# Kernel tuning notes

Hardware: AMD Instinct MI355X
Metric: run time of the kernel (lower is better)

The kernel has to match this reference:

```python
import jax, jax.numpy as jnp
import numpy as np

N_PATIENT = 50000
N_GENE = 20000
N_EDGE = 640000
P_DIM, G_DIM, H, OUT = 64, 32, 128, 8


def setup_inputs() -> dict:
    key = jax.random.key(0)
    ks = jax.random.split(key, 20)
    s = 0.02
    return {
        "x_patient": jax.random.normal(ks[0], (N_PATIENT, P_DIM), jnp.float32),
        "x_gene": jax.random.normal(ks[1], (N_GENE, G_DIM), jnp.float32),
        "edge_index": jax.random.randint(ks[2], (2, N_EDGE), 0, N_GENE, jnp.int32),
        # patient MLP
        "W_p1": jax.random.normal(ks[3], (P_DIM, H), jnp.float32) * s,
        "b_p1": jnp.zeros((H,), jnp.float32),
        "W_p2": jax.random.normal(ks[4], (H, H), jnp.float32) * s,
        "b_p2": jnp.zeros((H,), jnp.float32),
        # gene MLP
        "W_g1": jax.random.normal(ks[5], (G_DIM, H), jnp.float32) * s,
        "b_g1": jnp.zeros((H,), jnp.float32),
        "W_g2": jax.random.normal(ks[6], (H, H), jnp.float32) * s,
        "b_g2": jnp.zeros((H,), jnp.float32),
        # SAGEConv 1: lin_l acts on aggregated src, lin_r (root) on dst
        "W1_l": jax.random.normal(ks[7], (H, H), jnp.float32) * s,
        "b1_l": jnp.zeros((H,), jnp.float32),
        "W1_r": jax.random.normal(ks[8], (H, H), jnp.float32) * s,
        # SAGEConv 2
        "W2_l": jax.random.normal(ks[9], (H, H), jnp.float32) * s,
        "b2_l": jnp.zeros((H,), jnp.float32),
        "W2_r": jax.random.normal(ks[10], (H, H), jnp.float32) * s,
        # final fc
        "W_fc": jax.random.normal(ks[11], (H, OUT), jnp.float32) * s,
        "b_fc": jnp.zeros((OUT,), jnp.float32),
    }


def reference(x_patient, x_gene, edge_index,
              W_p1, b_p1, W_p2, b_p2,
              W_g1, b_g1, W_g2, b_g2,
              W1_l, b1_l, W1_r,
              W2_l, b2_l, W2_r,
              W_fc, b_fc):
    # node-type MLPs
    p = jax.nn.relu(x_patient @ W_p1 + b_p1) @ W_p2 + b_p2   # [N_P, H]
    g = jax.nn.relu(x_gene @ W_g1 + b_g1) @ W_g2 + b_g2       # [N_G, H]

    src, dst = edge_index[0], edge_index[1]
    # gene_x is unchanged between layers, so the sum-aggregate is identical
    # for both SAGEConv layers: compute the gather + segment-sum once.
    agg = jax.ops.segment_sum(g[src], dst, num_segments=x_patient.shape[0])  # [N_P, H]

    # SAGEConv(aggr='sum'): out = lin_l(agg) + lin_r(x_dst), bias in lin_l
    p = jax.nn.relu(agg @ W1_l + b1_l + p @ W1_r)
    p = jax.nn.relu(agg @ W2_l + b2_l + p @ W2_r)
    return p @ W_fc + b_fc  # [N_P, OUT]
```

## Files before the change

kernel.cpp:

```cpp
#include <hip/hip_runtime.h>

#define NP 50000
#define NG 20000
#define NE 640000
#define PD 64
#define GD 32
#define HD 128
#define OD 8
#define CAP 96
#define FILLB 125
#define EPB 5120
#define GENE_TILES 313
#define ROW0_NOAGG 20096
#define PAT2B 234
#define SAGE64B 314
#define AGGPAD (ROW0_NOAGG - NG)

using f32x4 = __attribute__((ext_vector_type(4))) float;
using s16x8 = __attribute__((ext_vector_type(8))) short;

__device__ __forceinline__ unsigned short f2bf(float f) {
    union { float f; unsigned u; } v; v.f = f;
    const unsigned r = v.u + 0x7FFFu + ((v.u >> 16) & 1u);
    return (unsigned short)(r >> 16);
}
__device__ __forceinline__ float bfpair_lo(unsigned v) {
    union { unsigned u; float f; } x; x.u = v << 16; return x.f;
}
__device__ __forceinline__ float bfpair_hi(unsigned v) {
    union { unsigned u; float f; } x; x.u = v & 0xFFFF0000u; return x.f;
}

#define TOT_SWZ 112640

__global__ __launch_bounds__(256) void swz_kernel(
    const float* __restrict__ Wp1, const float* __restrict__ Wp2,
    const float* __restrict__ W1l, const float* __restrict__ W1r,
    const float* __restrict__ W2l, const float* __restrict__ W2r,
    const float* __restrict__ Wfc,
    const float* __restrict__ Wg1, const float* __restrict__ Wg2,
    unsigned short* __restrict__ wswz, unsigned short* __restrict__ aggb)
{
    const int u = blockIdx.x * 256 + threadIdx.x;
    if (u < TOT_SWZ) {
        const float* src; int K, Nr, doff;
        if      (u <   8192) { src = Wp1; K =  64; Nr = HD; doff = 0; }
        else if (u <  24576) { src = Wp2; K = 128; Nr = HD; doff = 8192; }
        else if (u <  40960) { src = W1l; K = 128; Nr = HD; doff = 24576; }
        else if (u <  57344) { src = W1r; K = 128; Nr = HD; doff = 40960; }
        else if (u <  73728) { src = W2l; K = 128; Nr = HD; doff = 57344; }
        else if (u <  90112) { src = W2r; K = 128; Nr = HD; doff = 73728; }
        else if (u <  92160) { src = Wfc; K = 128; Nr = OD; doff = 90112; }
        else if (u <  96256) { src = Wg1; K =  32; Nr = HD; doff = 92160; }
        else                 { src = Wg2; K = 128; Nr = HD; doff = 96256; }
        const int e  = u - doff;
        const int j  = e & 7;
        const int ln = (e >> 3) & 63;
        const int f  = e >> 9;
        const int KC = K >> 5;
        const int c  = f % KC;
        const int n0 = f / KC;
        const int k  = c * 32 + (ln >> 4) * 8 + j;
        const int n  = n0 * 16 + (ln & 15);
        wswz[u] = f2bf((n < Nr) ? src[k * Nr + n] : 0.f);
    } else {
        aggb[(size_t)NG * HD + (u - TOT_SWZ)] = 0;
    }
}

__global__ __launch_bounds__(256) void genefill_kernel(
    const float* __restrict__ xg,
    const unsigned short* __restrict__ wswz,
    const float* __restrict__ bg1, const float* __restrict__ bg2,
    unsigned short* __restrict__ g,
    const int* __restrict__ ei, unsigned short* __restrict__ hist16)
{
    __shared__ __align__(16) char smem[20480];
    const int tid = threadIdx.x;
    if (blockIdx.x >= GENE_TILES) {
        int* cnt = (int*)smem;
#pragma unroll
        for (int k = 0; k < 5; ++k) {
            const int idx = k * 256 + tid;
            if (idx < NG / 16) ((int4*)cnt)[idx] = (int4){0, 0, 0, 0};
        }
        __syncthreads();
        const int fb = blockIdx.x - GENE_TILES;
        const int base = fb * EPB;
#pragma unroll
        for (int it = 0; it < 5; ++it) {
            const int e0 = base + it * 1024 + tid;
            const int d0 = ei[NE + e0];
            const int d1 = ei[NE + e0 + 256];
            const int d2 = ei[NE + e0 + 512];
            const int d3 = ei[NE + e0 + 768];
            atomicAdd(&cnt[d0 >> 2], 1 << ((d0 & 3) * 8));
            atomicAdd(&cnt[d1 >> 2], 1 << ((d1 & 3) * 8));
            atomicAdd(&cnt[d2 >> 2], 1 << ((d2 & 3) * 8));
            atomicAdd(&cnt[d3 >> 2], 1 << ((d3 & 3) * 8));
        }
        __syncthreads();
        unsigned short* Hb = hist16 + fb * NG;
#pragma unroll
        for (int k = 0; k < 20; ++k) {
            const int idx = k * 256 + tid;
            if (idx < NG / 4) {
                const unsigned w = (unsigned)cnt[idx];
                int2 o;
                o.x = (int)((w & 0xFFu) | ((w & 0xFF00u) << 8));
                o.y = (int)(((w >> 16) & 0xFFu) | (((w >> 24) & 0xFFu) << 16));
                ((int2*)Hb)[idx] = o;
            }
        }
        return;
    }
    const unsigned short* wg1 = wswz + 92160;
    const unsigned short* wg2 = wswz + 96256;

    const int lane = tid & 63;
    const int wid  = tid >> 6;
    const int quad = lane >> 4;
    const int l16  = lane & 15;
    const int row0 = blockIdx.x * 64 + wid * 16;
    const int arow = min(row0 + l16, NG - 1);
    unsigned short* X = (unsigned short*)smem + wid * 16 * 136;
    const f32x4 Z = {0.f, 0.f, 0.f, 0.f};

    s16x8 a;
    {
        const float* xr = xg + (size_t)arow * GD + quad * 8;
        const f32x4 u0 = *(const f32x4*)xr;
        const f32x4 u1 = *(const f32x4*)(xr + 4);
#pragma unroll
        for (int j = 0; j < 4; ++j) {
            a[j]     = (short)f2bf(u0[j]);
            a[4 + j] = (short)f2bf(u1[j]);
        }
    }
    f32x4 C[8];
#pragma unroll
    for (int n = 0; n < 8; ++n) {
        const s16x8 b = *(const s16x8*)&wg1[(n * 64 + lane) * 8];
        C[n] = __builtin_amdgcn_mfma_f32_16x16x32_bf16(a, b, Z, 0, 0, 0);
    }
#pragma unroll
    for (int n = 0; n < 8; ++n) {
        const float bias = bg1[n * 16 + l16];
#pragma unroll
        for (int r = 0; r < 4; ++r)
            X[(quad * 4 + r) * 136 + n * 16 + l16] = f2bf(fmaxf(C[n][r] + bias, 0.f));
    }
    __syncthreads();
    s16x8 pa[4];
#pragma unroll
    for (int c = 0; c < 4; ++c) pa[c] = *(const s16x8*)&X[l16 * 136 + c * 32 + quad * 8];
#pragma unroll
    for (int n = 0; n < 8; ++n) {
        C[n] = Z;
#pragma unroll
        for (int c = 0; c < 4; ++c) {
            const s16x8 b = *(const s16x8*)&wg2[((n * 4 + c) * 64 + lane) * 8];
            C[n] = __builtin_amdgcn_mfma_f32_16x16x32_bf16(pa[c], b, C[n], 0, 0, 0);
        }
    }
#pragma unroll
    for (int n = 0; n < 8; ++n) {
        const float bias = bg2[n * 16 + l16];
#pragma unroll
        for (int r = 0; r < 4; ++r) {
            const int row = row0 + quad * 4 + r;
            if (row < NG) g[(size_t)row * HD + n * 16 + l16] = f2bf(C[n][r] + bias);
        }
    }
}

__global__ __launch_bounds__(256) void scan_kernel(
    unsigned short* __restrict__ hist16, int* __restrict__ cursor)
{
    const int d = blockIdx.x * 256 + threadIdx.x;
    if (d >= NG) return;
    int run = 0;
#pragma unroll 5
    for (int b = 0; b < FILLB; ++b) {
        const int t = hist16[b * NG + d];
        hist16[b * NG + d] = (unsigned short)run;
        run += t;
    }
    cursor[d] = run;
}

__global__ __launch_bounds__(256) void placepat_kernel(
    const int* __restrict__ ei, const unsigned short* __restrict__ hist16,
    unsigned short* __restrict__ pad,
    const float* __restrict__ xp, const unsigned short* __restrict__ wswz,
    const float* __restrict__ bp1, const float* __restrict__ bp2,
    const float* __restrict__ b1l, const float* __restrict__ b2l,
    const float* __restrict__ bfc,
    float* __restrict__ out)
{
    __shared__ __align__(16) char smem[40960];
    const int tid = threadIdx.x;

    if (blockIdx.x < FILLB) {
        int* cnt = (int*)smem;
        const int* Hb = (const int*)(hist16 + blockIdx.x * NG);
#pragma unroll
        for (int k = 0; k < 10; ++k) {
            const int idx = k * 256 + tid;
            if (idx < NG / 8) ((int4*)cnt)[idx] = ((const int4*)Hb)[idx];
        }
        __syncthreads();
        const int base = blockIdx.x * EPB;
#pragma unroll
        for (int it = 0; it < 5; ++it) {
            const int e0 = base + it * 1024 + tid;
            const int s0 = ei[e0];       const int d0 = ei[NE + e0];
            const int s1 = ei[e0 + 256]; const int d1 = ei[NE + e0 + 256];
            const int s2 = ei[e0 + 512]; const int d2 = ei[NE + e0 + 512];
            const int s3 = ei[e0 + 768]; const int d3 = ei[NE + e0 + 768];
            { const int o = atomicAdd(&cnt[d0 >> 1], 1 << ((d0 & 1) * 16));
              const int p = (o >> ((d0 & 1) * 16)) & 0xFFFF;
              if (p < CAP) pad[d0 * CAP + p] = (unsigned short)s0; }
            { const int o = atomicAdd(&cnt[d1 >> 1], 1 << ((d1 & 1) * 16));
              const int p = (o >> ((d1 & 1) * 16)) & 0xFFFF;
              if (p < CAP) pad[d1 * CAP + p] = (unsigned short)s1; }
            { const int o = atomicAdd(&cnt[d2 >> 1], 1 << ((d2 & 1) * 16));
              const int p = (o >> ((d2 & 1) * 16)) & 0xFFFF;
              if (p < CAP) pad[d2 * CAP + p] = (unsigned short)s2; }
            { const int o = atomicAdd(&cnt[d3 >> 1], 1 << ((d3 & 1) * 16));
              const int p = (o >> ((d3 & 1) * 16)) & 0xFFFF;
              if (p < CAP) pad[d3 * CAP + p] = (unsigned short)s3; }
        }
        return;
    }

    const unsigned short* wp1 = wswz + 0;
    const unsigned short* wp2 = wswz + 8192;
    const unsigned short* w1r = wswz + 40960;
    const unsigned short* w2r = wswz + 73728;
    const unsigned short* wfc = wswz + 90112;

    unsigned short* XA = (unsigned short*)smem;
    const int lane = tid & 63;
    const int wid  = tid >> 6;
    const int quad = lane >> 4;
    const int l16  = lane & 15;
    const int brow = ROW0_NOAGG + (blockIdx.x - FILLB) * 128;
    const int nA = wid * 2, nB = wid * 2 + 1;
    const f32x4 Z = {0.f, 0.f, 0.f, 0.f};

#pragma unroll
    for (int s = 0; s < 8; ++s) {
        const int slot = s * 256 + tid;
        const int r  = slot >> 4;
        const int cv = slot & 15;
        const f32x4 u = *(const f32x4*)&xp[(size_t)min(brow + r, NP - 1) * PD + cv * 4];
        unsigned short o[4];
#pragma unroll
        for (int j = 0; j < 4; ++j) o[j] = f2bf(u[j]);
        *(ushort4*)&XA[r * 136 + cv * 4] = *(ushort4*)o;
    }
    __syncthreads();

    f32x4 acc[8][2];

#pragma unroll
    for (int rt = 0; rt < 8; ++rt) { acc[rt][0] = Z; acc[rt][1] = Z; }
#pragma unroll
    for (int c = 0; c < 2; ++c) {
        const s16x8 b0 = *(const s16x8*)&wp1[((nA * 2 + c) * 64 + lane) * 8];
        const s16x8 b1 = *(const s16x8*)&wp1[((nB * 2 + c) * 64 + lane) * 8];
#pragma unroll
        for (int rt = 0; rt < 8; ++rt) {
            const s16x8 a = *(const s16x8*)&XA[(rt * 16 + l16) * 136 + c * 32 + quad * 8];
            acc[rt][0] = __builtin_amdgcn_mfma_f32_16x16x32_bf16(a, b0, acc[rt][0], 0, 0, 0);
            acc[rt][1] = __builtin_amdgcn_mfma_f32_16x16x32_bf16(a, b1, acc[rt][1], 0, 0, 0);
        }
    }
    __syncthreads();
#pragma unroll
    for (int t = 0; t < 2; ++t) {
        const int n = wid * 2 + t;
        const float bias = bp1[n * 16 + l16];
#pragma unroll
        for (int rt = 0; rt < 8; ++rt)
#pragma unroll
            for (int r = 0; r < 4; ++r)
                XA[(rt * 16 + quad * 4 + r) * 136 + n * 16 + l16] =
                    f2bf(fmaxf(acc[rt][t][r] + bias, 0.f));
    }
    __syncthreads();

#pragma unroll
    for (int rt = 0; rt < 8; ++rt) { acc[rt][0] = Z; acc[rt][1] = Z; }
#pragma unroll
    for (int c = 0; c < 4; ++c) {
        const s16x8 b0 = *(const s16x8*)&wp2[((nA * 4 + c) * 64 + lane) * 8];
        const s16x8 b1 = *(const s16x8*)&wp2[((nB * 4 + c) * 64 + lane) * 8];
#pragma unroll
        for (int rt = 0; rt < 8; ++rt) {
            const s16x8 a = *(const s16x8*)&XA[(rt * 16 + l16) * 136 + c * 32 + quad * 8];
            acc[rt][0] = __builtin_amdgcn_mfma_f32_16x16x32_bf16(a, b0, acc[rt][0], 0, 0, 0);
            acc[rt][1] = __builtin_amdgcn_mfma_f32_16x16x32_bf16(a, b1, acc[rt][1], 0, 0, 0);
        }
    }
    __syncthreads();
#pragma unroll
    for (int t = 0; t < 2; ++t) {
        const int n = wid * 2 + t;
        const float bias = bp2[n * 16 + l16];
#pragma unroll
        for (int rt = 0; rt < 8; ++rt)
#pragma unroll
            for (int r = 0; r < 4; ++r)
                XA[(rt * 16 + quad * 4 + r) * 136 + n * 16 + l16] =
                    f2bf(acc[rt][t][r] + bias);
    }
    __syncthreads();

#pragma unroll
    for (int rt = 0; rt < 8; ++rt) { acc[rt][0] = Z; acc[rt][1] = Z; }
#pragma unroll
    for (int c = 0; c < 4; ++c) {
        const s16x8 b0 = *(const s16x8*)&w1r[((nA * 4 + c) * 64 + lane) * 8];
        const s16x8 b1 = *(const s16x8*)&w1r[((nB * 4 + c) * 64 + lane) * 8];
#pragma unroll
        for (int rt = 0; rt < 8; ++rt) {
            const s16x8 a = *(const s16x8*)&XA[(rt * 16 + l16) * 136 + c * 32 + quad * 8];
            acc[rt][0] = __builtin_amdgcn_mfma_f32_16x16x32_bf16(a, b0, acc[rt][0], 0, 0, 0);
            acc[rt][1] = __builtin_amdgcn_mfma_f32_16x16x32_bf16(a, b1, acc[rt][1], 0, 0, 0);
        }
    }
    __syncthreads();
#pragma unroll
    for (int t = 0; t < 2; ++t) {
        const int n = wid * 2 + t;
        const float bias = b1l[n * 16 + l16];
#pragma unroll
        for (int rt = 0; rt < 8; ++rt)
#pragma unroll
            for (int r = 0; r < 4; ++r)
                XA[(rt * 16 + quad * 4 + r) * 136 + n * 16 + l16] =
                    f2bf(fmaxf(acc[rt][t][r] + bias, 0.f));
    }
    __syncthreads();

#pragma unroll
    for (int rt = 0; rt < 8; ++rt) { acc[rt][0] = Z; acc[rt][1] = Z; }
#pragma unroll
    for (int c = 0; c < 4; ++c) {
        const s16x8 b0 = *(const s16x8*)&w2r[((nA * 4 + c) * 64 + lane) * 8];
        const s16x8 b1 = *(const s16x8*)&w2r[((nB * 4 + c) * 64 + lane) * 8];
#pragma unroll
        for (int rt = 0; rt < 8; ++rt) {
            const s16x8 a = *(const s16x8*)&XA[(rt * 16 + l16) * 136 + c * 32 + quad * 8];
            acc[rt][0] = __builtin_amdgcn_mfma_f32_16x16x32_bf16(a, b0, acc[rt][0], 0, 0, 0);
            acc[rt][1] = __builtin_amdgcn_mfma_f32_16x16x32_bf16(a, b1, acc[rt][1], 0, 0, 0);
        }
    }
    __syncthreads();
#pragma unroll
    for (int t = 0; t < 2; ++t) {
        const int n = wid * 2 + t;
        const float bias = b2l[n * 16 + l16];
#pragma unroll
        for (int rt = 0; rt < 8; ++rt)
#pragma unroll
            for (int r = 0; r < 4; ++r)
                XA[(rt * 16 + quad * 4 + r) * 136 + n * 16 + l16] =
                    f2bf(fmaxf(acc[rt][t][r] + bias, 0.f));
    }
    __syncthreads();

    {
        f32x4 co[2] = {Z, Z};
#pragma unroll
        for (int c = 0; c < 4; ++c) {
            const s16x8 b = *(const s16x8*)&wfc[(c * 64 + lane) * 8];
#pragma unroll
            for (int j = 0; j < 2; ++j) {
                const int rt = wid * 2 + j;
                const s16x8 a = *(const s16x8*)&XA[(rt * 16 + l16) * 136 + c * 32 + quad * 8];
                co[j] = __builtin_amdgcn_mfma_f32_16x16x32_bf16(a, b, co[j], 0, 0, 0);
            }
        }
        if (l16 < OD) {
            const float bias = bfc[l16];
#pragma unroll
            for (int j = 0; j < 2; ++j)
#pragma unroll
                for (int r = 0; r < 4; ++r) {
                    const int row = brow + (wid * 2 + j) * 16 + quad * 4 + r;
                    if (row < NP) out[(size_t)row * OD + l16] = co[j][r] + bias;
                }
        }
    }
}

__global__ __launch_bounds__(256) void agg_kernel(
    const int* __restrict__ cursor, const unsigned short* __restrict__ pad,
    const unsigned short* __restrict__ g, unsigned short* __restrict__ aggb)
{
    const int row  = blockIdx.x * 4 + (threadIdx.x >> 6);
    const int lane = threadIdx.x & 63;
    const int grp  = lane >> 4;
    const int sub  = lane & 15;

    float acc[8] = {0.f, 0.f, 0.f, 0.f, 0.f, 0.f, 0.f, 0.f};
    const int cnt = min(cursor[row], CAP);
    const size_t rb = (size_t)row * CAP;
    for (int i = grp * 4; i < cnt; i += 16) {
        const ushort4 q = *(const ushort4*)&pad[rb + i];
        int r0 = q.x, r1 = q.y, r2 = q.z, r3 = q.w;
        const bool v1 = (i + 1) < cnt, v2 = (i + 2) < cnt, v3 = (i + 3) < cnt;
        r1 = v1 ? r1 : r0;  r2 = v2 ? r2 : r0;  r3 = v3 ? r3 : r0;
        const float s1 = v1 ? 1.f : 0.f, s2 = v2 ? 1.f : 0.f, s3 = v3 ? 1.f : 0.f;
        const s16x8 g0 = *(const s16x8*)&g[(size_t)r0 * HD + sub * 8];
        const s16x8 g1 = *(const s16x8*)&g[(size_t)r1 * HD + sub * 8];
        const s16x8 g2 = *(const s16x8*)&g[(size_t)r2 * HD + sub * 8];
        const s16x8 g3 = *(const s16x8*)&g[(size_t)r3 * HD + sub * 8];
        const unsigned* d0 = (const unsigned*)&g0;
        const unsigned* d1 = (const unsigned*)&g1;
        const unsigned* d2 = (const unsigned*)&g2;
        const unsigned* d3 = (const unsigned*)&g3;
#pragma unroll
        for (int k = 0; k < 4; ++k) {
            acc[2 * k]     += bfpair_lo(d0[k]);
            acc[2 * k + 1] += bfpair_hi(d0[k]);
            acc[2 * k]     = fmaf(bfpair_lo(d1[k]), s1, acc[2 * k]);
            acc[2 * k + 1] = fmaf(bfpair_hi(d1[k]), s1, acc[2 * k + 1]);
            acc[2 * k]     = fmaf(bfpair_lo(d2[k]), s2, acc[2 * k]);
            acc[2 * k + 1] = fmaf(bfpair_hi(d2[k]), s2, acc[2 * k + 1]);
            acc[2 * k]     = fmaf(bfpair_lo(d3[k]), s3, acc[2 * k]);
            acc[2 * k + 1] = fmaf(bfpair_hi(d3[k]), s3, acc[2 * k + 1]);
        }
    }
#pragma unroll
    for (int k = 0; k < 8; ++k) {
        acc[k] += __shfl_xor(acc[k], 16);
        acc[k] += __shfl_xor(acc[k], 32);
    }
    if (lane < 16) {
        unsigned o[4];
#pragma unroll
        for (int k = 0; k < 4; ++k)
            o[k] = (unsigned)f2bf(acc[2 * k]) | ((unsigned)f2bf(acc[2 * k + 1]) << 16);
        *(int4*)&aggb[(size_t)row * HD + lane * 8] = *(int4*)o;
    }
}

__global__ __launch_bounds__(256) void sage64_kernel(
    const float* __restrict__ xp, const unsigned short* __restrict__ aggb,
    const unsigned short* __restrict__ wswz,
    const float* __restrict__ bp1, const float* __restrict__ bp2,
    const float* __restrict__ b1l, const float* __restrict__ b2l,
    const float* __restrict__ bfc,
    float* __restrict__ out)
{
    const unsigned short* wp1 = wswz + 0;
    const unsigned short* wp2 = wswz + 8192;
    const unsigned short* w1l = wswz + 24576;
    const unsigned short* w1r = wswz + 40960;
    const unsigned short* w2l = wswz + 57344;
    const unsigned short* w2r = wswz + 73728;
    const unsigned short* wfc = wswz + 90112;

    __shared__ __align__(16) unsigned short XA[64 * 136];

    const int tid  = threadIdx.x;
    const int lane = tid & 63;
    const int wid  = tid >> 6;
    const int quad = lane >> 4;
    const int l16  = lane & 15;
    const int brow = blockIdx.x * 64;
    const int nA = wid * 2, nB = wid * 2 + 1;
    const f32x4 Z = {0.f, 0.f, 0.f, 0.f};

#pragma unroll
    for (int s = 0; s < 4; ++s) {
        const int slot = s * 256 + tid;
        const int r  = slot >> 4;
        const int cv = slot & 15;
        const f32x4 u = *(const f32x4*)&xp[(size_t)(brow + r) * PD + cv * 4];
        unsigned short o[4];
#pragma unroll
        for (int j = 0; j < 4; ++j) o[j] = f2bf(u[j]);
        *(ushort4*)&XA[r * 136 + cv * 4] = *(ushort4*)o;
    }
    __syncthreads();

    f32x4 acc[4][2];

#pragma unroll
    for (int rt = 0; rt < 4; ++rt) { acc[rt][0] = Z; acc[rt][1] = Z; }
#pragma unroll
    for (int c = 0; c < 2; ++c) {
        const s16x8 b0 = *(const s16x8*)&wp1[((nA * 2 + c) * 64 + lane) * 8];
        const s16x8 b1 = *(const s16x8*)&wp1[((nB * 2 + c) * 64 + lane) * 8];
#pragma unroll
        for (int rt = 0; rt < 4; ++rt) {
            const s16x8 a = *(const s16x8*)&XA[(rt * 16 + l16) * 136 + c * 32 + quad * 8];
            acc[rt][0] = __builtin_amdgcn_mfma_f32_16x16x32_bf16(a, b0, acc[rt][0], 0, 0, 0);
            acc[rt][1] = __builtin_amdgcn_mfma_f32_16x16x32_bf16(a, b1, acc[rt][1], 0, 0, 0);
        }
    }
    __syncthreads();
#pragma unroll
    for (int t = 0; t < 2; ++t) {
        const int n = wid * 2 + t;
        const float bias = bp1[n * 16 + l16];
#pragma unroll
        for (int rt = 0; rt < 4; ++rt)
#pragma unroll
            for (int r = 0; r < 4; ++r)
                XA[(rt * 16 + quad * 4 + r) * 136 + n * 16 + l16] =
                    f2bf(fmaxf(acc[rt][t][r] + bias, 0.f));
    }
    __syncthreads();

#pragma unroll
    for (int rt = 0; rt < 4; ++rt) { acc[rt][0] = Z; acc[rt][1] = Z; }
#pragma unroll
    for (int c = 0; c < 4; ++c) {
        const s16x8 b0 = *(const s16x8*)&wp2[((nA * 4 + c) * 64 + lane) * 8];
        const s16x8 b1 = *(const s16x8*)&wp2[((nB * 4 + c) * 64 + lane) * 8];
#pragma unroll
        for (int rt = 0; rt < 4; ++rt) {
            const s16x8 a = *(const s16x8*)&XA[(rt * 16 + l16) * 136 + c * 32 + quad * 8];
            acc[rt][0] = __builtin_amdgcn_mfma_f32_16x16x32_bf16(a, b0, acc[rt][0], 0, 0, 0);
            acc[rt][1] = __builtin_amdgcn_mfma_f32_16x16x32_bf16(a, b1, acc[rt][1], 0, 0, 0);
        }
    }
    __syncthreads();
#pragma unroll
    for (int t = 0; t < 2; ++t) {
        const int n = wid * 2 + t;
        const float bias = bp2[n * 16 + l16];
#pragma unroll
        for (int rt = 0; rt < 4; ++rt)
#pragma unroll
            for (int r = 0; r < 4; ++r)
                XA[(rt * 16 + quad * 4 + r) * 136 + n * 16 + l16] =
                    f2bf(acc[rt][t][r] + bias);
    }
    __syncthreads();

#pragma unroll
    for (int rt = 0; rt < 4; ++rt) { acc[rt][0] = Z; acc[rt][1] = Z; }
#pragma unroll
    for (int c = 0; c < 4; ++c) {
        const s16x8 br0 = *(const s16x8*)&w1r[((nA * 4 + c) * 64 + lane) * 8];
        const s16x8 br1 = *(const s16x8*)&w1r[((nB * 4 + c) * 64 + lane) * 8];
        const s16x8 bl0 = *(const s16x8*)&w1l[((nA * 4 + c) * 64 + lane) * 8];
        const s16x8 bl1 = *(const s16x8*)&w1l[((nB * 4 + c) * 64 + lane) * 8];
#pragma unroll
        for (int rt = 0; rt < 4; ++rt) {
            const s16x8 ap = *(const s16x8*)&XA[(rt * 16 + l16) * 136 + c * 32 + quad * 8];
            const s16x8 ag = *(const s16x8*)&aggb[(size_t)(brow + rt * 16 + l16) * HD + c * 32 + quad * 8];
            acc[rt][0] = __builtin_amdgcn_mfma_f32_16x16x32_bf16(ap, br0, acc[rt][0], 0, 0, 0);
            acc[rt][0] = __builtin_amdgcn_mfma_f32_16x16x32_bf16(ag, bl0, acc[rt][0], 0, 0, 0);
            acc[rt][1] = __builtin_amdgcn_mfma_f32_16x16x32_bf16(ap, br1, acc[rt][1], 0, 0, 0);
            acc[rt][1] = __builtin_amdgcn_mfma_f32_16x16x32_bf16(ag, bl1, acc[rt][1], 0, 0, 0);
        }
    }
    __syncthreads();
#pragma unroll
    for (int t = 0; t < 2; ++t) {
        const int n = wid * 2 + t;
        const float bias = b1l[n * 16 + l16];
#pragma unroll
        for (int rt = 0; rt < 4; ++rt)
#pragma unroll
            for (int r = 0; r < 4; ++r)
                XA[(rt * 16 + quad * 4 + r) * 136 + n * 16 + l16] =
                    f2bf(fmaxf(acc[rt][t][r] + bias, 0.f));
    }
    __syncthreads();

#pragma unroll
    for (int rt = 0; rt < 4; ++rt) { acc[rt][0] = Z; acc[rt][1] = Z; }
#pragma unroll
    for (int c = 0; c < 4; ++c) {
        const s16x8 br0 = *(const s16x8*)&w2r[((nA * 4 + c) * 64 + lane) * 8];
        const s16x8 br1 = *(const s16x8*)&w2r[((nB * 4 + c) * 64 + lane) * 8];
        const s16x8 bl0 = *(const s16x8*)&w2l[((nA * 4 + c) * 64 + lane) * 8];
        const s16x8 bl1 = *(const s16x8*)&w2l[((nB * 4 + c) * 64 + lane) * 8];
#pragma unroll
        for (int rt = 0; rt < 4; ++rt) {
            const s16x8 ap = *(const s16x8*)&XA[(rt * 16 + l16) * 136 + c * 32 + quad * 8];
            const s16x8 ag = *(const s16x8*)&aggb[(size_t)(brow + rt * 16 + l16) * HD + c * 32 + quad * 8];
            acc[rt][0] = __builtin_amdgcn_mfma_f32_16x16x32_bf16(ap, br0, acc[rt][0], 0, 0, 0);
            acc[rt][0] = __builtin_amdgcn_mfma_f32_16x16x32_bf16(ag, bl0, acc[rt][0], 0, 0, 0);
            acc[rt][1] = __builtin_amdgcn_mfma_f32_16x16x32_bf16(ap, br1, acc[rt][1], 0, 0, 0);
            acc[rt][1] = __builtin_amdgcn_mfma_f32_16x16x32_bf16(ag, bl1, acc[rt][1], 0, 0, 0);
        }
    }
    __syncthreads();
#pragma unroll
    for (int t = 0; t < 2; ++t) {
        const int n = wid * 2 + t;
        const float bias = b2l[n * 16 + l16];
#pragma unroll
        for (int rt = 0; rt < 4; ++rt)
#pragma unroll
            for (int r = 0; r < 4; ++r)
                XA[(rt * 16 + quad * 4 + r) * 136 + n * 16 + l16] =
                    f2bf(fmaxf(acc[rt][t][r] + bias, 0.f));
    }
    __syncthreads();

    {
        f32x4 co = Z;
#pragma unroll
        for (int c = 0; c < 4; ++c) {
            const s16x8 b = *(const s16x8*)&wfc[(c * 64 + lane) * 8];
            const s16x8 a = *(const s16x8*)&XA[(wid * 16 + l16) * 136 + c * 32 + quad * 8];
            co = __builtin_amdgcn_mfma_f32_16x16x32_bf16(a, b, co, 0, 0, 0);
        }
        if (l16 < OD) {
            const float bias = bfc[l16];
#pragma unroll
            for (int r = 0; r < 4; ++r) {
                const int row = brow + wid * 16 + quad * 4 + r;
                out[(size_t)row * OD + l16] = co[r] + bias;
            }
        }
    }
}

extern "C" void kernel_launch(void* const* d_in, const int* in_sizes, int n_in,
                              void* d_out, int out_size, void* d_ws, size_t ws_size,
                              hipStream_t stream)
{
    const float* xp  = (const float*)d_in[0];
    const float* xg  = (const float*)d_in[1];
    const int*   ei  = (const int*)d_in[2];
    const float* Wp1 = (const float*)d_in[3];
    const float* bp1 = (const float*)d_in[4];
    const float* Wp2 = (const float*)d_in[5];
    const float* bp2 = (const float*)d_in[6];
    const float* Wg1 = (const float*)d_in[7];
    const float* bg1 = (const float*)d_in[8];
    const float* Wg2 = (const float*)d_in[9];
    const float* bg2 = (const float*)d_in[10];
    const float* W1l = (const float*)d_in[11];
    const float* b1l = (const float*)d_in[12];
    const float* W1r = (const float*)d_in[13];
    const float* W2l = (const float*)d_in[14];
    const float* b2l = (const float*)d_in[15];
    const float* W2r = (const float*)d_in[16];
    const float* Wfc = (const float*)d_in[17];
    const float* bfc = (const float*)d_in[18];
    float* out = (float*)d_out;

    char* ws = (char*)d_ws;
    unsigned short* g_b    = (unsigned short*)(ws + 0);
    unsigned short* wswz   = (unsigned short*)(ws + 5120000);
    int*            cursor = (int*)(ws + 5345280);
    unsigned short* hist16 = (unsigned short*)(ws + 5425280);
    unsigned short* pad    = (unsigned short*)(ws + 10425280);
    unsigned short* agg_b  = (unsigned short*)(ws + 14265280);

    swz_kernel<<<(TOT_SWZ + AGGPAD * HD) / 256, 256, 0, stream>>>(
        Wp1, Wp2, W1l, W1r, W2l, W2r, Wfc, Wg1, Wg2, wswz, agg_b);

    genefill_kernel<<<GENE_TILES + FILLB, 256, 0, stream>>>(
        xg, wswz, bg1, bg2, g_b, ei, hist16);

    scan_kernel<<<(NG + 255) / 256, 256, 0, stream>>>(hist16, cursor);

    placepat_kernel<<<FILLB + PAT2B, 256, 0, stream>>>(
        ei, hist16, pad, xp, wswz, bp1, bp2, b1l, b2l, bfc, out);

    agg_kernel<<<NG / 4, 256, 0, stream>>>(cursor, pad, g_b, agg_b);

    sage64_kernel<<<SAGE64B, 256, 0, stream>>>(
        xp, agg_b, wswz, bp1, bp2, b1l, b2l, bfc, out);
}
```

Measured before the change: 174.0 us.

## Fuse all stages into one cooperative persistent kernel with grid syncs

Replaces the six separate kernel launches with a single cooperative mega-kernel that walks phases (weight swizzle, gene MLP plus histogram plus the non-aggregated patient rows, scan plus patient precompute, edge placement, aggregation, SAGE) separated by grid-wide barriers. The histogram work is also re-split into more, smaller edge blocks, and the patient MLP output is staged in a bf16 buffer. The aim is to remove launch gaps and tail idling between dependent stages. In exchange it adds grid-sync cost, caps occupancy through the launch bound, and keeps a multi-launch fallback path in case the cooperative launch fails.

```diff
diff --git a/kernel.cpp b/kernel.cpp
--- a/kernel.cpp
+++ b/kernel.cpp
@@ -1,4 +1,7 @@
 #include <hip/hip_runtime.h>
+#include <hip/hip_cooperative_groups.h>
+
+namespace cg = cooperative_groups;
 
 #define NP 50000
 #define NG 20000
@@ -8,13 +11,21 @@
 #define HD 128
 #define OD 8
 #define CAP 96
-#define FILLB 125
-#define EPB 5120
-#define GENE_TILES 313
-#define ROW0_NOAGG 20096
-#define PAT2B 234
-#define SAGE64B 314
-#define AGGPAD (ROW0_NOAGG - NG)
+#define FILLB 250
+#define EPB 2560
+
+#define GENE_ITEMS 313
+#define NOAGG0 20032
+#define NOAGG_ITEMS 469
+#define P1_ITEMS (FILLB + GENE_ITEMS + NOAGG_ITEMS)
+#define SCAN_ITEMS 79
+#define PCOMP_ITEMS 313
+#define P2_ITEMS (SCAN_ITEMS + PCOMP_ITEMS)
+#define AGG_ITEMS (NG / 4)
+#define SAGE_ITEMS 313
+#define AGGPAD 32
+#define TOT_SWZ 112640
+#define SMEM_BYTES 40960
 
 using f32x4 = __attribute__((ext_vector_type(4))) float;
 using s16x8 = __attribute__((ext_vector_type(8))) short;
@@ -31,432 +42,37 @@
     union { unsigned u; float f; } x; x.u = v & 0xFFFF0000u; return x.f;
 }
 
-#define TOT_SWZ 112640
-
-__global__ __launch_bounds__(256) void swz_kernel(
+__global__ __launch_bounds__(256, 4) void mega_kernel(
+    const float* __restrict__ xp, const float* __restrict__ xg,
+    const int* __restrict__ ei,
+    const float* __restrict__ bp1, const float* __restrict__ bp2,
+    const float* __restrict__ b1l, const float* __restrict__ b2l,
+    const float* __restrict__ bfc,
+    const float* __restrict__ bg1, const float* __restrict__ bg2,
     const float* __restrict__ Wp1, const float* __restrict__ Wp2,
     const float* __restrict__ W1l, const float* __restrict__ W1r,
     const float* __restrict__ W2l, const float* __restrict__ W2r,
-    const float* __restrict__ Wfc,
-    const float* __restrict__ Wg1, const float* __restrict__ Wg2,
-    unsigned short* __restrict__ wswz, unsigned short* __restrict__ aggb)
+    const float* __restrict__ Wfc, const float* __restrict__ Wg1,
+    const float* __restrict__ Wg2,
+    unsigned short* __restrict__ wswz, unsigned short* __restrict__ g,
+    unsigned short* __restrict__ hist16, int* __restrict__ cursor,
+    unsigned short* __restrict__ pad, unsigned short* __restrict__ p_b,
+    unsigned short* __restrict__ aggb, float* __restrict__ out,
+    int phase_lo, int phase_hi)
 {
-    const int u = blockIdx.x * 256 + threadIdx.x;
-    if (u < TOT_SWZ) {
-        const float* src; int K, Nr, doff;
-        if      (u <   8192) { src = Wp1; K =  64; Nr = HD; doff = 0; }
-        else if (u <  24576) { src = Wp2; K = 128; Nr = HD; doff = 8192; }
-        else if (u <  40960) { src = W1l; K = 128; Nr = HD; doff = 24576; }
-        else if (u <  57344) { src = W1r; K = 128; Nr = HD; doff = 40960; }
-        else if (u <  73728) { src = W2l; K = 128; Nr = HD; doff = 57344; }
-        else if (u <  90112) { src = W2r; K = 128; Nr = HD; doff = 73728; }
-        else if (u <  92160) { src = Wfc; K = 128; Nr = OD; doff = 90112; }
-        else if (u <  96256) { src = Wg1; K =  32; Nr = HD; doff = 92160; }
-        else                 { src = Wg2; K = 128; Nr = HD; doff = 96256; }
-        const int e  = u - doff;
-        const int j  = e & 7;
-        const int ln = (e >> 3) & 63;
-        const int f  = e >> 9;
-        const int KC = K >> 5;
-        const int c  = f % KC;
-        const int n0 = f / KC;
-        const int k  = c * 32 + (ln >> 4) * 8 + j;
-        const int n  = n0 * 16 + (ln & 15);
-        wswz[u] = f2bf((n < Nr) ? src[k * Nr + n] : 0.f);
-    } else {
-        aggb[(size_t)NG * HD + (u - TOT_SWZ)] = 0;
-    }
-}
-
-__global__ __launch_bounds__(256) void genefill_kernel(
-    const float* __restrict__ xg,
-    const unsigned short* __restrict__ wswz,
-    const float* __restrict__ bg1, const float* __restrict__ bg2,
-    unsigned short* __restrict__ g,
-    const int* __restrict__ ei, unsigned short* __restrict__ hist16)
-{
-    __shared__ __align__(16) char smem[20480];
-    const int tid = threadIdx.x;
-    if (blockIdx.x >= GENE_TILES) {
-        int* cnt = (int*)smem;
-#pragma unroll
-        for (int k = 0; k < 5; ++k) {
-            const int idx = k * 256 + tid;
-            if (idx < NG / 16) ((int4*)cnt)[idx] = (int4){0, 0, 0, 0};
-        }
-        __syncthreads();
-        const int fb = blockIdx.x - GENE_TILES;
-        const int base = fb * EPB;
-#pragma unroll
-        for (int it = 0; it < 5; ++it) {
-            const int e0 = base + it * 1024 + tid;
-            const int d0 = ei[NE + e0];
-            const int d1 = ei[NE + e0 + 256];
-            const int d2 = ei[NE + e0 + 512];
-            const int d3 = ei[NE + e0 + 768];
-            atomicAdd(&cnt[d0 >> 2], 1 << ((d0 & 3) * 8));
-            atomicAdd(&cnt[d1 >> 2], 1 << ((d1 & 3) * 8));
-            atomicAdd(&cnt[d2 >> 2], 1 << ((d2 & 3) * 8));
-            atomicAdd(&cnt[d3 >> 2], 1 << ((d3 & 3) * 8));
-        }
-        __syncthreads();
-        unsigned short* Hb = hist16 + fb * NG;
-#pragma unroll
-        for (int k = 0; k < 20; ++k) {
-            const int idx = k * 256 + tid;
-            if (idx < NG / 4) {
-                const unsigned w = (unsigned)cnt[idx];
-                int2 o;
-                o.x = (int)((w & 0xFFu) | ((w & 0xFF00u) << 8));
-                o.y = (int)(((w >> 16) & 0xFFu) | (((w >> 24) & 0xFFu) << 16));
-                ((int2*)Hb)[idx] = o;
-            }
-        }
-        return;
-    }
-    const unsigned short* wg1 = wswz + 92160;
-    const unsigned short* wg2 = wswz + 96256;
-
+    cg::grid_group grid = cg::this_grid();
+    extern __shared__ int4 smem4[];
+    char* smem = (char*)smem4;
+    const bool coop = (phase_lo != phase_hi);
+    const int G   = gridDim.x;
+    const int bid = blockIdx.x;
+    const int tid  = threadIdx.x;
     const int lane = tid & 63;
     const int wid  = tid >> 6;
     const int quad = lane >> 4;
     const int l16  = lane & 15;
-    const int row0 = blockIdx.x * 64 + wid * 16;
-    const int arow = min(row0 + l16, NG - 1);
-    unsigned short* X = (unsigned short*)smem + wid * 16 * 136;
     const f32x4 Z = {0.f, 0.f, 0.f, 0.f};
 
-    s16x8 a;
-    {
-        const float* xr = xg + (size_t)arow * GD + quad * 8;
-        const f32x4 u0 = *(const f32x4*)xr;
-        const f32x4 u1 = *(const f32x4*)(xr + 4);
-#pragma unroll
-        for (int j = 0; j < 4; ++j) {
-            a[j]     = (short)f2bf(u0[j]);
-            a[4 + j] = (short)f2bf(u1[j]);
-        }
-    }
-    f32x4 C[8];
-#pragma unroll
-    for (int n = 0; n < 8; ++n) {
-        const s16x8 b = *(const s16x8*)&wg1[(n * 64 + lane) * 8];
-        C[n] = __builtin_amdgcn_mfma_f32_16x16x32_bf16(a, b, Z, 0, 0, 0);
-    }
-#pragma unroll
-    for (int n = 0; n < 8; ++n) {
-        const float bias = bg1[n * 16 + l16];
-#pragma unroll
-        for (int r = 0; r < 4; ++r)
-            X[(quad * 4 + r) * 136 + n * 16 + l16] = f2bf(fmaxf(C[n][r] + bias, 0.f));
-    }
-    __syncthreads();
-    s16x8 pa[4];
-#pragma unroll
-    for (int c = 0; c < 4; ++c) pa[c] = *(const s16x8*)&X[l16 * 136 + c * 32 + quad * 8];
-#pragma unroll
-    for (int n = 0; n < 8; ++n) {
-        C[n] = Z;
-#pragma unroll
-        for (int c = 0; c < 4; ++c) {
-            const s16x8 b = *(const s16x8*)&wg2[((n * 4 + c) * 64 + lane) * 8];
-            C[n] = __builtin_amdgcn_mfma_f32_16x16x32_bf16(pa[c], b, C[n], 0, 0, 0);
-        }
-    }
-#pragma unroll
-    for (int n = 0; n < 8; ++n) {
-        const float bias = bg2[n * 16 + l16];
-#pragma unroll
-        for (int r = 0; r < 4; ++r) {
-            const int row = row0 + quad * 4 + r;
-            if (row < NG) g[(size_t)row * HD + n * 16 + l16] = f2bf(C[n][r] + bias);
-        }
-    }
-}
-
-__global__ __launch_bounds__(256) void scan_kernel(
-    unsigned short* __restrict__ hist16, int* __restrict__ cursor)
-{
-    const int d = blockIdx.x * 256 + threadIdx.x;
-    if (d >= NG) return;
-    int run = 0;
-#pragma unroll 5
-    for (int b = 0; b < FILLB; ++b) {
-        const int t = hist16[b * NG + d];
-        hist16[b * NG + d] = (unsigned short)run;
-        run += t;
-    }
-    cursor[d] = run;
-}
-
-__global__ __launch_bounds__(256) void placepat_kernel(
-    const int* __restrict__ ei, const unsigned short* __restrict__ hist16,
-    unsigned short* __restrict__ pad,
-    const float* __restrict__ xp, const unsigned short* __restrict__ wswz,
-    const float* __restrict__ bp1, const float* __restrict__ bp2,
-    const float* __restrict__ b1l, const float* __restrict__ b2l,
-    const float* __restrict__ bfc,
-    float* __restrict__ out)
-{
-    __shared__ __align__(16) char smem[40960];
-    const int tid = threadIdx.x;
-
-    if (blockIdx.x < FILLB) {
-        int* cnt = (int*)smem;
-        const int* Hb = (const int*)(hist16 + blockIdx.x * NG);
-#pragma unroll
-        for (int k = 0; k < 10; ++k) {
-            const int idx = k * 256 + tid;
-            if (idx < NG / 8) ((int4*)cnt)[idx] = ((const int4*)Hb)[idx];
-        }
-        __syncthreads();
-        const int base = blockIdx.x * EPB;
-#pragma unroll
-        for (int it = 0; it < 5; ++it) {
-            const int e0 = base + it * 1024 + tid;
-            const int s0 = ei[e0];       const int d0 = ei[NE + e0];
-            const int s1 = ei[e0 + 256]; const int d1 = ei[NE + e0 + 256];
-            const int s2 = ei[e0 + 512]; const int d2 = ei[NE + e0 + 512];
-            const int s3 = ei[e0 + 768]; const int d3 = ei[NE + e0 + 768];
-            { const int o = atomicAdd(&cnt[d0 >> 1], 1 << ((d0 & 1) * 16));
-              const int p = (o >> ((d0 & 1) * 16)) & 0xFFFF;
-              if (p < CAP) pad[d0 * CAP + p] = (unsigned short)s0; }
-            { const int o = atomicAdd(&cnt[d1 >> 1], 1 << ((d1 & 1) * 16));
-              const int p = (o >> ((d1 & 1) * 16)) & 0xFFFF;
-              if (p < CAP) pad[d1 * CAP + p] = (unsigned short)s1; }
-            { const int o = atomicAdd(&cnt[d2 >> 1], 1 << ((d2 & 1) * 16));
-              const int p = (o >> ((d2 & 1) * 16)) & 0xFFFF;
-              if (p < CAP) pad[d2 * CAP + p] = (unsigned short)s2; }
-            { const int o = atomicAdd(&cnt[d3 >> 1], 1 << ((d3 & 1) * 16));
-              const int p = (o >> ((d3 & 1) * 16)) & 0xFFFF;
-              if (p < CAP) pad[d3 * CAP + p] = (unsigned short)s3; }
-        }
-        return;
-    }
-
-    const unsigned short* wp1 = wswz + 0;
-    const unsigned short* wp2 = wswz + 8192;
-    const unsigned short* w1r = wswz + 40960;
-    const unsigned short* w2r = wswz + 73728;
-    const unsigned short* wfc = wswz + 90112;
-
-    unsigned short* XA = (unsigned short*)smem;
-    const int lane = tid & 63;
-    const int wid  = tid >> 6;
-    const int quad = lane >> 4;
-    const int l16  = lane & 15;
-    const int brow = ROW0_NOAGG + (blockIdx.x - FILLB) * 128;
-    const int nA = wid * 2, nB = wid * 2 + 1;
-    const f32x4 Z = {0.f, 0.f, 0.f, 0.f};
-
-#pragma unroll
-    for (int s = 0; s < 8; ++s) {
-        const int slot = s * 256 + tid;
-        const int r  = slot >> 4;
-        const int cv = slot & 15;
-        const f32x4 u = *(const f32x4*)&xp[(size_t)min(brow + r, NP - 1) * PD + cv * 4];
-        unsigned short o[4];
-#pragma unroll
-        for (int j = 0; j < 4; ++j) o[j] = f2bf(u[j]);
-        *(ushort4*)&XA[r * 136 + cv * 4] = *(ushort4*)o;
-    }
-    __syncthreads();
-
-    f32x4 acc[8][2];
-
-#pragma unroll
-    for (int rt = 0; rt < 8; ++rt) { acc[rt][0] = Z; acc[rt][1] = Z; }
-#pragma unroll
-    for (int c = 0; c < 2; ++c) {
-        const s16x8 b0 = *(const s16x8*)&wp1[((nA * 2 + c) * 64 + lane) * 8];
-        const s16x8 b1 = *(const s16x8*)&wp1[((nB * 2 + c) * 64 + lane) * 8];
-#pragma unroll
-        for (int rt = 0; rt < 8; ++rt) {
-            const s16x8 a = *(const s16x8*)&XA[(rt * 16 + l16) * 136 + c * 32 + quad * 8];
-            acc[rt][0] = __builtin_amdgcn_mfma_f32_16x16x32_bf16(a, b0, acc[rt][0], 0, 0, 0);
-            acc[rt][1] = __builtin_amdgcn_mfma_f32_16x16x32_bf16(a, b1, acc[rt][1], 0, 0, 0);
-        }
-    }
-    __syncthreads();
-#pragma unroll
-    for (int t = 0; t < 2; ++t) {
-        const int n = wid * 2 + t;
-        const float bias = bp1[n * 16 + l16];
-#pragma unroll
-        for (int rt = 0; rt < 8; ++rt)
-#pragma unroll
-            for (int r = 0; r < 4; ++r)
-                XA[(rt * 16 + quad * 4 + r) * 136 + n * 16 + l16] =
-                    f2bf(fmaxf(acc[rt][t][r] + bias, 0.f));
-    }
-    __syncthreads();
-
-#pragma unroll
-    for (int rt = 0; rt < 8; ++rt) { acc[rt][0] = Z; acc[rt][1] = Z; }
-#pragma unroll
-    for (int c = 0; c < 4; ++c) {
-        const s16x8 b0 = *(const s16x8*)&wp2[((nA * 4 + c) * 64 + lane) * 8];
-        const s16x8 b1 = *(const s16x8*)&wp2[((nB * 4 + c) * 64 + lane) * 8];
-#pragma unroll
-        for (int rt = 0; rt < 8; ++rt) {
-            const s16x8 a = *(const s16x8*)&XA[(rt * 16 + l16) * 136 + c * 32 + quad * 8];
-            acc[rt][0] = __builtin_amdgcn_mfma_f32_16x16x32_bf16(a, b0, acc[rt][0], 0, 0, 0);
-            acc[rt][1] = __builtin_amdgcn_mfma_f32_16x16x32_bf16(a, b1, acc[rt][1], 0, 0, 0);
-        }
-    }
-    __syncthreads();
-#pragma unroll
-    for (int t = 0; t < 2; ++t) {
-        const int n = wid * 2 + t;
-        const float bias = bp2[n * 16 + l16];
-#pragma unroll
-        for (int rt = 0; rt < 8; ++rt)
-#pragma unroll
-            for (int r = 0; r < 4; ++r)
-                XA[(rt * 16 + quad * 4 + r) * 136 + n * 16 + l16] =
-                    f2bf(acc[rt][t][r] + bias);
-    }
-    __syncthreads();
-
-#pragma unroll
-    for (int rt = 0; rt < 8; ++rt) { acc[rt][0] = Z; acc[rt][1] = Z; }
-#pragma unroll
-    for (int c = 0; c < 4; ++c) {
-        const s16x8 b0 = *(const s16x8*)&w1r[((nA * 4 + c) * 64 + lane) * 8];
-        const s16x8 b1 = *(const s16x8*)&w1r[((nB * 4 + c) * 64 + lane) * 8];
-#pragma unroll
-        for (int rt = 0; rt < 8; ++rt) {
-            const s16x8 a = *(const s16x8*)&XA[(rt * 16 + l16) * 136 + c * 32 + quad * 8];
-            acc[rt][0] = __builtin_amdgcn_mfma_f32_16x16x32_bf16(a, b0, acc[rt][0], 0, 0, 0);
-            acc[rt][1] = __builtin_amdgcn_mfma_f32_16x16x32_bf16(a, b1, acc[rt][1], 0, 0, 0);
-        }
-    }
-    __syncthreads();
-#pragma unroll
-    for (int t = 0; t < 2; ++t) {
-        const int n = wid * 2 + t;
-        const float bias = b1l[n * 16 + l16];
-#pragma unroll
-        for (int rt = 0; rt < 8; ++rt)
-#pragma unroll
-            for (int r = 0; r < 4; ++r)
-                XA[(rt * 16 + quad * 4 + r) * 136 + n * 16 + l16] =
-                    f2bf(fmaxf(acc[rt][t][r] + bias, 0.f));
-    }
-    __syncthreads();
-
-#pragma unroll
-    for (int rt = 0; rt < 8; ++rt) { acc[rt][0] = Z; acc[rt][1] = Z; }
-#pragma unroll
-    for (int c = 0; c < 4; ++c) {
-        const s16x8 b0 = *(const s16x8*)&w2r[((nA * 4 + c) * 64 + lane) * 8];
-        const s16x8 b1 = *(const s16x8*)&w2r[((nB * 4 + c) * 64 + lane) * 8];
-#pragma unroll
-        for (int rt = 0; rt < 8; ++rt) {
-            const s16x8 a = *(const s16x8*)&XA[(rt * 16 + l16) * 136 + c * 32 + quad * 8];
-            acc[rt][0] = __builtin_amdgcn_mfma_f32_16x16x32_bf16(a, b0, acc[rt][0], 0, 0, 0);
-            acc[rt][1] = __builtin_amdgcn_mfma_f32_16x16x32_bf16(a, b1, acc[rt][1], 0, 0, 0);
-        }
-    }
-    __syncthreads();
-#pragma unroll
-    for (int t = 0; t < 2; ++t) {
-        const int n = wid * 2 + t;
-        const float bias = b2l[n * 16 + l16];
-#pragma unroll
-        for (int rt = 0; rt < 8; ++rt)
-#pragma unroll
-            for (int r = 0; r < 4; ++r)
-                XA[(rt * 16 + quad * 4 + r) * 136 + n * 16 + l16] =
-                    f2bf(fmaxf(acc[rt][t][r] + bias, 0.f));
-    }
-    __syncthreads();
-
-    {
-        f32x4 co[2] = {Z, Z};
-#pragma unroll
-        for (int c = 0; c < 4; ++c) {
-            const s16x8 b = *(const s16x8*)&wfc[(c * 64 + lane) * 8];
-#pragma unroll
-            for (int j = 0; j < 2; ++j) {
-                const int rt = wid * 2 + j;
-                const s16x8 a = *(const s16x8*)&XA[(rt * 16 + l16) * 136 + c * 32 + quad * 8];
-                co[j] = __builtin_amdgcn_mfma_f32_16x16x32_bf16(a, b, co[j], 0, 0, 0);
-            }
-        }
-        if (l16 < OD) {
-            const float bias = bfc[l16];
-#pragma unroll
-            for (int j = 0; j < 2; ++j)
-#pragma unroll
-                for (int r = 0; r < 4; ++r) {
-                    const int row = brow + (wid * 2 + j) * 16 + quad * 4 + r;
-                    if (row < NP) out[(size_t)row * OD + l16] = co[j][r] + bias;
-                }
-        }
-    }
-}
-
-__global__ __launch_bounds__(256) void agg_kernel(
-    const int* __restrict__ cursor, const unsigned short* __restrict__ pad,
-    const unsigned short* __restrict__ g, unsigned short* __restrict__ aggb)
-{
-    const int row  = blockIdx.x * 4 + (threadIdx.x >> 6);
-    const int lane = threadIdx.x & 63;
-    const int grp  = lane >> 4;
-    const int sub  = lane & 15;
-
-    float acc[8] = {0.f, 0.f, 0.f, 0.f, 0.f, 0.f, 0.f, 0.f};
-    const int cnt = min(cursor[row], CAP);
-    const size_t rb = (size_t)row * CAP;
-    for (int i = grp * 4; i < cnt; i += 16) {
-        const ushort4 q = *(const ushort4*)&pad[rb + i];
-        int r0 = q.x, r1 = q.y, r2 = q.z, r3 = q.w;
-        const bool v1 = (i + 1) < cnt, v2 = (i + 2) < cnt, v3 = (i + 3) < cnt;
-        r1 = v1 ? r1 : r0;  r2 = v2 ? r2 : r0;  r3 = v3 ? r3 : r0;
-        const float s1 = v1 ? 1.f : 0.f, s2 = v2 ? 1.f : 0.f, s3 = v3 ? 1.f : 0.f;
-        const s16x8 g0 = *(const s16x8*)&g[(size_t)r0 * HD + sub * 8];
-        const s16x8 g1 = *(const s16x8*)&g[(size_t)r1 * HD + sub * 8];
-        const s16x8 g2 = *(const s16x8*)&g[(size_t)r2 * HD + sub * 8];
-        const s16x8 g3 = *(const s16x8*)&g[(size_t)r3 * HD + sub * 8];
-        const unsigned* d0 = (const unsigned*)&g0;
-        const unsigned* d1 = (const unsigned*)&g1;
-        const unsigned* d2 = (const unsigned*)&g2;
-        const unsigned* d3 = (const unsigned*)&g3;
-#pragma unroll
-        for (int k = 0; k < 4; ++k) {
-            acc[2 * k]     += bfpair_lo(d0[k]);
-            acc[2 * k + 1] += bfpair_hi(d0[k]);
-            acc[2 * k]     = fmaf(bfpair_lo(d1[k]), s1, acc[2 * k]);
-            acc[2 * k + 1] = fmaf(bfpair_hi(d1[k]), s1, acc[2 * k + 1]);
-            acc[2 * k]     = fmaf(bfpair_lo(d2[k]), s2, acc[2 * k]);
-            acc[2 * k + 1] = fmaf(bfpair_hi(d2[k]), s2, acc[2 * k + 1]);
-            acc[2 * k]     = fmaf(bfpair_lo(d3[k]), s3, acc[2 * k]);
-            acc[2 * k + 1] = fmaf(bfpair_hi(d3[k]), s3, acc[2 * k + 1]);
-        }
-    }
-#pragma unroll
-    for (int k = 0; k < 8; ++k) {
-        acc[k] += __shfl_xor(acc[k], 16);
-        acc[k] += __shfl_xor(acc[k], 32);
-    }
-    if (lane < 16) {
-        unsigned o[4];
-#pragma unroll
-        for (int k = 0; k < 4; ++k)
-            o[k] = (unsigned)f2bf(acc[2 * k]) | ((unsigned)f2bf(acc[2 * k + 1]) << 16);
-        *(int4*)&aggb[(size_t)row * HD + lane * 8] = *(int4*)o;
-    }
-}
-
-__global__ __launch_bounds__(256) void sage64_kernel(
-    const float* __restrict__ xp, const unsigned short* __restrict__ aggb,
-    const unsigned short* __restrict__ wswz,
-    const float* __restrict__ bp1, const float* __restrict__ bp2,
-    const float* __restrict__ b1l, const float* __restrict__ b2l,
-    const float* __restrict__ bfc,
-    float* __restrict__ out)
-{
     const unsigned short* wp1 = wswz + 0;
     const unsigned short* wp2 = wswz + 8192;
     const unsigned short* w1l = wswz + 24576;
@@ -464,167 +80,520 @@
     const unsigned short* w2l = wswz + 57344;
     const unsigned short* w2r = wswz + 73728;
     const unsigned short* wfc = wswz + 90112;
-
-    __shared__ __align__(16) unsigned short XA[64 * 136];
-
-    const int tid  = threadIdx.x;
-    const int lane = tid & 63;
-    const int wid  = tid >> 6;
-    const int quad = lane >> 4;
-    const int l16  = lane & 15;
-    const int brow = blockIdx.x * 64;
-    const int nA = wid * 2, nB = wid * 2 + 1;
-    const f32x4 Z = {0.f, 0.f, 0.f, 0.f};
-
-#pragma unroll
-    for (int s = 0; s < 4; ++s) {
-        const int slot = s * 256 + tid;
-        const int r  = slot >> 4;
-        const int cv = slot & 15;
-        const f32x4 u = *(const f32x4*)&xp[(size_t)(brow + r) * PD + cv * 4];
-        unsigned short o[4];
-#pragma unroll
-        for (int j = 0; j < 4; ++j) o[j] = f2bf(u[j]);
-        *(ushort4*)&XA[r * 136 + cv * 4] = *(ushort4*)o;
-    }
-    __syncthreads();
-
-    f32x4 acc[4][2];
-
-#pragma unroll
-    for (int rt = 0; rt < 4; ++rt) { acc[rt][0] = Z; acc[rt][1] = Z; }
-#pragma unroll
-    for (int c = 0; c < 2; ++c) {
-        const s16x8 b0 = *(const s16x8*)&wp1[((nA * 2 + c) * 64 + lane) * 8];
-        const s16x8 b1 = *(const s16x8*)&wp1[((nB * 2 + c) * 64 + lane) * 8];
-#pragma unroll
-        for (int rt = 0; rt < 4; ++rt) {
-            const s16x8 a = *(const s16x8*)&XA[(rt * 16 + l16) * 136 + c * 32 + quad * 8];
-            acc[rt][0] = __builtin_amdgcn_mfma_f32_16x16x32_bf16(a, b0, acc[rt][0], 0, 0, 0);
-            acc[rt][1] = __builtin_amdgcn_mfma_f32_16x16x32_bf16(a, b1, acc[rt][1], 0, 0, 0);
-        }
-    }
-    __syncthreads();
-#pragma unroll
-    for (int t = 0; t < 2; ++t) {
-        const int n = wid * 2 + t;
-        const float bias = bp1[n * 16 + l16];
-#pragma unroll
-        for (int rt = 0; rt < 4; ++rt)
-#pragma unroll
-            for (int r = 0; r < 4; ++r)
-                XA[(rt * 16 + quad * 4 + r) * 136 + n * 16 + l16] =
-                    f2bf(fmaxf(acc[rt][t][r] + bias, 0.f));
-    }
-    __syncthreads();
-
-#pragma unroll
-    for (int rt = 0; rt < 4; ++rt) { acc[rt][0] = Z; acc[rt][1] = Z; }
-#pragma unroll
-    for (int c = 0; c < 4; ++c) {
-        const s16x8 b0 = *(const s16x8*)&wp2[((nA * 4 + c) * 64 + lane) * 8];
-        const s16x8 b1 = *(const s16x8*)&wp2[((nB * 4 + c) * 64 + lane) * 8];
-#pragma unroll
-        for (int rt = 0; rt < 4; ++rt) {
-            const s16x8 a = *(const s16x8*)&XA[(rt * 16 + l16) * 136 + c * 32 + quad * 8];
-            acc[rt][0] = __builtin_amdgcn_mfma_f32_16x16x32_bf16(a, b0, acc[rt][0], 0, 0, 0);
-            acc[rt][1] = __builtin_amdgcn_mfma_f32_16x16x32_bf16(a, b1, acc[rt][1], 0, 0, 0);
-        }
-    }
-    __syncthreads();
-#pragma unroll
-    for (int t = 0; t < 2; ++t) {
-        const int n = wid * 2 + t;
-        const float bias = bp2[n * 16 + l16];
-#pragma unroll
-        for (int rt = 0; rt < 4; ++rt)
-#pragma unroll
-            for (int r = 0; r < 4; ++r)
-                XA[(rt * 16 + quad * 4 + r) * 136 + n * 16 + l16] =
-                    f2bf(acc[rt][t][r] + bias);
-    }
-    __syncthreads();
-
-#pragma unroll
-    for (int rt = 0; rt < 4; ++rt) { acc[rt][0] = Z; acc[rt][1] = Z; }
-#pragma unroll
-    for (int c = 0; c < 4; ++c) {
-        const s16x8 br0 = *(const s16x8*)&w1r[((nA * 4 + c) * 64 + lane) * 8];
-        const s16x8 br1 = *(const s16x8*)&w1r[((nB * 4 + c) * 64 + lane) * 8];
-        const s16x8 bl0 = *(const s16x8*)&w1l[((nA * 4 + c) * 64 + lane) * 8];
-        const s16x8 bl1 = *(const s16x8*)&w1l[((nB * 4 + c) * 64 + lane) * 8];
-#pragma unroll
-        for (int rt = 0; rt < 4; ++rt) {
-            const s16x8 ap = *(const s16x8*)&XA[(rt * 16 + l16) * 136 + c * 32 + quad * 8];
-            const s16x8 ag = *(const s16x8*)&aggb[(size_t)(brow + rt * 16 + l16) * HD + c * 32 + quad * 8];
-            acc[rt][0] = __builtin_amdgcn_mfma_f32_16x16x32_bf16(ap, br0, acc[rt][0], 0, 0, 0);
-            acc[rt][0] = __builtin_amdgcn_mfma_f32_16x16x32_bf16(ag, bl0, acc[rt][0], 0, 0, 0);
-            acc[rt][1] = __builtin_amdgcn_mfma_f32_16x16x32_bf16(ap, br1, acc[rt][1], 0, 0, 0);
-            acc[rt][1] = __builtin_amdgcn_mfma_f32_16x16x32_bf16(ag, bl1, acc[rt][1], 0, 0, 0);
-        }
-    }
-    __syncthreads();
-#pragma unroll
-    for (int t = 0; t < 2; ++t) {
-        const int n = wid * 2 + t;
-        const float bias = b1l[n * 16 + l16];
-#pragma unroll
-        for (int rt = 0; rt < 4; ++rt)
-#pragma unroll
-            for (int r = 0; r < 4; ++r)
-                XA[(rt * 16 + quad * 4 + r) * 136 + n * 16 + l16] =
-                    f2bf(fmaxf(acc[rt][t][r] + bias, 0.f));
-    }
-    __syncthreads();
-
-#pragma unroll
-    for (int rt = 0; rt < 4; ++rt) { acc[rt][0] = Z; acc[rt][1] = Z; }
-#pragma unroll
-    for (int c = 0; c < 4; ++c) {
-        const s16x8 br0 = *(const s16x8*)&w2r[((nA * 4 + c) * 64 + lane) * 8];
-        const s16x8 br1 = *(const s16x8*)&w2r[((nB * 4 + c) * 64 + lane) * 8];
-        const s16x8 bl0 = *(const s16x8*)&w2l[((nA * 4 + c) * 64 + lane) * 8];
-        const s16x8 bl1 = *(const s16x8*)&w2l[((nB * 4 + c) * 64 + lane) * 8];
-#pragma unroll
-        for (int rt = 0; rt < 4; ++rt) {
-            const s16x8 ap = *(const s16x8*)&XA[(rt * 16 + l16) * 136 + c * 32 + quad * 8];
-            const s16x8 ag = *(const s16x8*)&aggb[(size_t)(brow + rt * 16 + l16) * HD + c * 32 + quad * 8];
-            acc[rt][0] = __builtin_amdgcn_mfma_f32_16x16x32_bf16(ap, br0, acc[rt][0], 0, 0, 0);
-            acc[rt][0] = __builtin_amdgcn_mfma_f32_16x16x32_bf16(ag, bl0, acc[rt][0], 0, 0, 0);
-            acc[rt][1] = __builtin_amdgcn_mfma_f32_16x16x32_bf16(ap, br1, acc[rt][1], 0, 0, 0);
-            acc[rt][1] = __builtin_amdgcn_mfma_f32_16x16x32_bf16(ag, bl1, acc[rt][1], 0, 0, 0);
-        }
-    }
-    __syncthreads();
-#pragma unroll
-    for (int t = 0; t < 2; ++t) {
-        const int n = wid * 2 + t;
-        const float bias = b2l[n * 16 + l16];
-#pragma unroll
-        for (int rt = 0; rt < 4; ++rt)
-#pragma unroll
-            for (int r = 0; r < 4; ++r)
-                XA[(rt * 16 + quad * 4 + r) * 136 + n * 16 + l16] =
-                    f2bf(fmaxf(acc[rt][t][r] + bias, 0.f));
-    }
-    __syncthreads();
-
-    {
-        f32x4 co = Z;
+    const unsigned short* wg1 = wswz + 92160;
+    const unsigned short* wg2 = wswz + 96256;
+
+    if (phase_lo <= 0 && 0 <= phase_hi) {
+        for (int u = bid * 256 + tid; u < TOT_SWZ + AGGPAD * HD; u += G * 256) {
+            if (u < TOT_SWZ) {
+                const float* src; int K, Nr, doff;
+                if      (u <   8192) { src = Wp1; K =  64; Nr = HD; doff = 0; }
+                else if (u <  24576) { src = Wp2; K = 128; Nr = HD; doff = 8192; }
+                else if (u <  40960) { src = W1l; K = 128; Nr = HD; doff = 24576; }
+                else if (u <  57344) { src = W1r; K = 128; Nr = HD; doff = 40960; }
+                else if (u <  73728) { src = W2l; K = 128; Nr = HD; doff = 57344; }
+                else if (u <  90112) { src = W2r; K = 128; Nr = HD; doff = 73728; }
+                else if (u <  92160) { src = Wfc; K = 128; Nr = OD; doff = 90112; }
+                else if (u <  96256) { src = Wg1; K =  32; Nr = HD; doff = 92160; }
+                else                 { src = Wg2; K = 128; Nr = HD; doff = 96256; }
+                const int e  = u - doff;
+                const int j  = e & 7;
+                const int ln = (e >> 3) & 63;
+                const int f  = e >> 9;
+                const int KC = K >> 5;
+                const int c  = f % KC;
+                const int n0 = f / KC;
+                const int k  = c * 32 + (ln >> 4) * 8 + j;
+                const int n  = n0 * 16 + (ln & 15);
+                wswz[u] = f2bf((n < Nr) ? src[k * Nr + n] : 0.f);
+            } else {
+                aggb[(size_t)NG * HD + (u - TOT_SWZ)] = 0;
+            }
+        }
+    }
+    if (coop) grid.sync();
+
+    if (phase_lo <= 1 && 1 <= phase_hi) {
+    for (int it = bid; it < P1_ITEMS; it += G) {
+        __syncthreads();
+        if (it < FILLB) {
+            int* cnt = (int*)smem;
+#pragma unroll
+            for (int k2 = 0; k2 < 5; ++k2) {
+                const int idx = k2 * 256 + tid;
+                if (idx < NG / 16) ((int4*)cnt)[idx] = (int4){0, 0, 0, 0};
+            }
+            __syncthreads();
+            const int base = it * EPB;
+#pragma unroll
+            for (int it2 = 0; it2 < 10; ++it2) {
+                const int d0 = ei[NE + base + it2 * 256 + tid];
+                atomicAdd(&cnt[d0 >> 2], 1 << ((d0 & 3) * 8));
+            }
+            __syncthreads();
+            unsigned short* Hb = hist16 + it * NG;
+#pragma unroll
+            for (int k2 = 0; k2 < 20; ++k2) {
+                const int idx = k2 * 256 + tid;
+                if (idx < NG / 4) {
+                    const unsigned w = (unsigned)cnt[idx];
+                    int2 o;
+                    o.x = (int)((w & 0xFFu) | ((w & 0xFF00u) << 8));
+                    o.y = (int)(((w >> 16) & 0xFFu) | (((w >> 24) & 0xFFu) << 16));
+                    ((int2*)Hb)[idx] = o;
+                }
+            }
+        } else if (it < FILLB + GENE_ITEMS) {
+            const int tile = it - FILLB;
+            const int row0 = tile * 64 + wid * 16;
+            const int arow = min(row0 + l16, NG - 1);
+            unsigned short* X = (unsigned short*)smem + wid * 16 * 136;
+
+            s16x8 a;
+            {
+                const float* xr = xg + (size_t)arow * GD + quad * 8;
+                const f32x4 u0 = *(const f32x4*)xr;
+                const f32x4 u1 = *(const f32x4*)(xr + 4);
+#pragma unroll
+                for (int j = 0; j < 4; ++j) {
+                    a[j]     = (short)f2bf(u0[j]);
+                    a[4 + j] = (short)f2bf(u1[j]);
+                }
+            }
+            f32x4 C[8];
+#pragma unroll
+            for (int n = 0; n < 8; ++n) {
+                const s16x8 b = *(const s16x8*)&wg1[(n * 64 + lane) * 8];
+                C[n] = __builtin_amdgcn_mfma_f32_16x16x32_bf16(a, b, Z, 0, 0, 0);
+            }
+#pragma unroll
+            for (int n = 0; n < 8; ++n) {
+                const float bias = bg1[n * 16 + l16];
+#pragma unroll
+                for (int r = 0; r < 4; ++r)
+                    X[(quad * 4 + r) * 136 + n * 16 + l16] = f2bf(fmaxf(C[n][r] + bias, 0.f));
+            }
+            __syncthreads();
+            s16x8 pa[4];
+#pragma unroll
+            for (int c = 0; c < 4; ++c) pa[c] = *(const s16x8*)&X[l16 * 136 + c * 32 + quad * 8];
+#pragma unroll
+            for (int n = 0; n < 8; ++n) {
+                C[n] = Z;
+#pragma unroll
+                for (int c = 0; c < 4; ++c) {
+                    const s16x8 b = *(const s16x8*)&wg2[((n * 4 + c) * 64 + lane) * 8];
+                    C[n] = __builtin_amdgcn_mfma_f32_16x16x32_bf16(pa[c], b, C[n], 0, 0, 0);
+                }
+            }
+#pragma unroll
+            for (int n = 0; n < 8; ++n) {
+                const float bias = bg2[n * 16 + l16];
+#pragma unroll
+                for (int r = 0; r < 4; ++r) {
+                    const int row = row0 + quad * 4 + r;
+                    if (row < NG) g[(size_t)row * HD + n * 16 + l16] = f2bf(C[n][r] + bias);
+                }
+            }
+        } else {
+            const int nid  = it - (FILLB + GENE_ITEMS);
+            const int brow = NOAGG0 + nid * 64;
+            unsigned short* XA = (unsigned short*)smem;
+#pragma unroll
+            for (int s = 0; s < 4; ++s) {
+                const int slot = s * 256 + tid;
+                const int r  = slot >> 4;
+                const int cv = slot & 15;
+                const f32x4 u = *(const f32x4*)&xp[(size_t)min(brow + r, NP - 1) * PD + cv * 4];
+                unsigned short o[4];
+#pragma unroll
+                for (int j = 0; j < 4; ++j) o[j] = f2bf(u[j]);
+                *(ushort4*)&XA[r * 136 + cv * 4] = *(ushort4*)o;
+            }
+            __syncthreads();
+
+            f32x4 acc[4][2];
+#pragma unroll
+            for (int rt = 0; rt < 4; ++rt) { acc[rt][0] = Z; acc[rt][1] = Z; }
+#pragma unroll
+            for (int c = 0; c < 2; ++c) {
+                const s16x8 b0 = *(const s16x8*)&wp1[(((wid * 2) * 2 + c) * 64 + lane) * 8];
+                const s16x8 b1 = *(const s16x8*)&wp1[(((wid * 2 + 1) * 2 + c) * 64 + lane) * 8];
+#pragma unroll
+                for (int rt = 0; rt < 4; ++rt) {
+                    const s16x8 a = *(const s16x8*)&XA[(rt * 16 + l16) * 136 + c * 32 + quad * 8];
+                    acc[rt][0] = __builtin_amdgcn_mfma_f32_16x16x32_bf16(a, b0, acc[rt][0], 0, 0, 0);
+                    acc[rt][1] = __builtin_amdgcn_mfma_f32_16x16x32_bf16(a, b1, acc[rt][1], 0, 0, 0);
+                }
+            }
+            __syncthreads();
+#pragma unroll
+            for (int t = 0; t < 2; ++t) {
+                const int n = wid * 2 + t;
+                const float bias = bp1[n * 16 + l16];
+#pragma unroll
+                for (int rt = 0; rt < 4; ++rt)
+#pragma unroll
+                    for (int r = 0; r < 4; ++r)
+                        XA[(rt * 16 + quad * 4 + r) * 136 + n * 16 + l16] =
+                            f2bf(fmaxf(acc[rt][t][r] + bias, 0.f));
+            }
+            __syncthreads();
+#pragma unroll
+            for (int rt = 0; rt < 4; ++rt) { acc[rt][0] = Z; acc[rt][1] = Z; }
+#pragma unroll
+            for (int c = 0; c < 4; ++c) {
+                const s16x8 b0 = *(const s16x8*)&wp2[(((wid * 2) * 4 + c) * 64 + lane) * 8];
+                const s16x8 b1 = *(const s16x8*)&wp2[(((wid * 2 + 1) * 4 + c) * 64 + lane) * 8];
+#pragma unroll
+                for (int rt = 0; rt < 4; ++rt) {
+                    const s16x8 a = *(const s16x8*)&XA[(rt * 16 + l16) * 136 + c * 32 + quad * 8];
+                    acc[rt][0] = __builtin_amdgcn_mfma_f32_16x16x32_bf16(a, b0, acc[rt][0], 0, 0, 0);
+                    acc[rt][1] = __builtin_amdgcn_mfma_f32_16x16x32_bf16(a, b1, acc[rt][1], 0, 0, 0);
+                }
+            }
+            __syncthreads();
+#pragma unroll
+            for (int t = 0; t < 2; ++t) {
+                const int n = wid * 2 + t;
+                const float bias = bp2[n * 16 + l16];
+#pragma unroll
+                for (int rt = 0; rt < 4; ++rt)
+#pragma unroll
+                    for (int r = 0; r < 4; ++r)
+                        XA[(rt * 16 + quad * 4 + r) * 136 + n * 16 + l16] =
+                            f2bf(acc[rt][t][r] + bias);
+            }
+            __syncthreads();
+#pragma unroll
+            for (int rt = 0; rt < 4; ++rt) { acc[rt][0] = Z; acc[rt][1] = Z; }
+#pragma unroll
+            for (int c = 0; c < 4; ++c) {
+                const s16x8 b0 = *(const s16x8*)&w1r[(((wid * 2) * 4 + c) * 64 + lane) * 8];
+                const s16x8 b1 = *(const s16x8*)&w1r[(((wid * 2 + 1) * 4 + c) * 64 + lane) * 8];
+#pragma unroll
+                for (int rt = 0; rt < 4; ++rt) {
+                    const s16x8 a = *(const s16x8*)&XA[(rt * 16 + l16) * 136 + c * 32 + quad * 8];
+                    acc[rt][0] = __builtin_amdgcn_mfma_f32_16x16x32_bf16(a, b0, acc[rt][0], 0, 0, 0);
+                    acc[rt][1] = __builtin_amdgcn_mfma_f32_16x16x32_bf16(a, b1, acc[rt][1], 0, 0, 0);
+                }
+            }
+            __syncthreads();
+#pragma unroll
+            for (int t = 0; t < 2; ++t) {
+                const int n = wid * 2 + t;
+                const float bias = b1l[n * 16 + l16];
+#pragma unroll
+                for (int rt = 0; rt < 4; ++rt)
+#pragma unroll
+                    for (int r = 0; r < 4; ++r)
+                        XA[(rt * 16 + quad * 4 + r) * 136 + n * 16 + l16] =
+                            f2bf(fmaxf(acc[rt][t][r] + bias, 0.f));
+            }
+            __syncthreads();
+#pragma unroll
+            for (int rt = 0; rt < 4; ++rt) { acc[rt][0] = Z; acc[rt][1] = Z; }
+#pragma unroll
+            for (int c = 0; c < 4; ++c) {
+                const s16x8 b0 = *(const s16x8*)&w2r[(((wid * 2) * 4 + c) * 64 + lane) * 8];
+                const s16x8 b1 = *(const s16x8*)&w2r[(((wid * 2 + 1) * 4 + c) * 64 + lane) * 8];
+#pragma unroll
+                for (int rt = 0; rt < 4; ++rt) {
+                    const s16x8 a = *(const s16x8*)&XA[(rt * 16 + l16) * 136 + c * 32 + quad * 8];
+                    acc[rt][0] = __builtin_amdgcn_mfma_f32_16x16x32_bf16(a, b0, acc[rt][0], 0, 0, 0);
+                    acc[rt][1] = __builtin_amdgcn_mfma_f32_16x16x32_bf16(a, b1, acc[rt][1], 0, 0, 0);
+                }
+            }
+            __syncthreads();
+#pragma unroll
+            for (int t = 0; t < 2; ++t) {
+                const int n = wid * 2 + t;
+                const float bias = b2l[n * 16 + l16];
+#pragma unroll
+                for (int rt = 0; rt < 4; ++rt)
+#pragma unroll
+                    for (int r = 0; r < 4; ++r)
+                        XA[(rt * 16 + quad * 4 + r) * 136 + n * 16 + l16] =
+                            f2bf(fmaxf(acc[rt][t][r] + bias, 0.f));
+            }
+            __syncthreads();
+            {
+                f32x4 co = Z;
+#pragma unroll
+                for (int c = 0; c < 4; ++c) {
+                    const s16x8 b = *(const s16x8*)&wfc[(c * 64 + lane) * 8];
+                    const s16x8 a = *(const s16x8*)&XA[(wid * 16 + l16) * 136 + c * 32 + quad * 8];
+                    co = __builtin_amdgcn_mfma_f32_16x16x32_bf16(a, b, co, 0, 0, 0);
+                }
+                if (l16 < OD) {
+                    const float bias = bfc[l16];
+#pragma unroll
+                    for (int r = 0; r < 4; ++r) {
+                        const int row = brow + wid * 16 + quad * 4 + r;
+                        if (row < NP) out[(size_t)row * OD + l16] = co[r] + bias;
+                    }
+                }
+            }
+        }
+    }
+    }
+    if (coop) grid.sync();
+
+    if (phase_lo <= 2 && 2 <= phase_hi) {
+    for (int it = bid; it < P2_ITEMS; it += G) {
+        __syncthreads();
+        if (it < SCAN_ITEMS) {
+            const int d = it * 256 + tid;
+            if (d < NG) {
+                int run = 0;
+#pragma unroll 10
+                for (int b = 0; b < FILLB; ++b) {
+                    const int t = hist16[b * NG + d];
+                    hist16[b * NG + d] = (unsigned short)run;
+                    run += t;
+                }
+                cursor[d] = run;
+            }
+        } else {
+            const int brow = (it - SCAN_ITEMS) * 64;
+            unsigned short* XA = (unsigned short*)smem;
+#pragma unroll
+            for (int s = 0; s < 4; ++s) {
+                const int slot = s * 256 + tid;
+                const int r  = slot >> 4;
+                const int cv = slot & 15;
+                const f32x4 u = *(const f32x4*)&xp[(size_t)(brow + r) * PD + cv * 4];
+                unsigned short o[4];
+#pragma unroll
+                for (int j = 0; j < 4; ++j) o[j] = f2bf(u[j]);
+                *(ushort4*)&XA[r * 136 + cv * 4] = *(ushort4*)o;
+            }
+            __syncthreads();
+
+            f32x4 acc[4][2];
+#pragma unroll
+            for (int rt = 0; rt < 4; ++rt) { acc[rt][0] = Z; acc[rt][1] = Z; }
+#pragma unroll
+            for (int c = 0; c < 2; ++c) {
+                const s16x8 b0 = *(const s16x8*)&wp1[(((wid * 2) * 2 + c) * 64 + lane) * 8];
+                const s16x8 b1 = *(const s16x8*)&wp1[(((wid * 2 + 1) * 2 + c) * 64 + lane) * 8];
+#pragma unroll
+                for (int rt = 0; rt < 4; ++rt) {
+                    const s16x8 a = *(const s16x8*)&XA[(rt * 16 + l16) * 136 + c * 32 + quad * 8];
+                    acc[rt][0] = __builtin_amdgcn_mfma_f32_16x16x32_bf16(a, b0, acc[rt][0], 0, 0, 0);
+                    acc[rt][1] = __builtin_amdgcn_mfma_f32_16x16x32_bf16(a, b1, acc[rt][1], 0, 0, 0);
+                }
+            }
+            __syncthreads();
+#pragma unroll
+            for (int t = 0; t < 2; ++t) {
+                const int n = wid * 2 + t;
+                const float bias = bp1[n * 16 + l16];
+#pragma unroll
+                for (int rt = 0; rt < 4; ++rt)
+#pragma unroll
+                    for (int r = 0; r < 4; ++r)
+                        XA[(rt * 16 + quad * 4 + r) * 136 + n * 16 + l16] =
+                            f2bf(fmaxf(acc[rt][t][r] + bias, 0.f));
+            }
+            __syncthreads();
+#pragma unroll
+            for (int rt = 0; rt < 4; ++rt) { acc[rt][0] = Z; acc[rt][1] = Z; }
+#pragma unroll
+            for (int c = 0; c < 4; ++c) {
+                const s16x8 b0 = *(const s16x8*)&wp2[(((wid * 2) * 4 + c) * 64 + lane) * 8];
+                const s16x8 b1 = *(const s16x8*)&wp2[(((wid * 2 + 1) * 4 + c) * 64 + lane) * 8];
+#pragma unroll
+                for (int rt = 0; rt < 4; ++rt) {
+                    const s16x8 a = *(const s16x8*)&XA[(rt * 16 + l16) * 136 + c * 32 + quad * 8];
+                    acc[rt][0] = __builtin_amdgcn_mfma_f32_16x16x32_bf16(a, b0, acc[rt][0], 0, 0, 0);
+                    acc[rt][1] = __builtin_amdgcn_mfma_f32_16x16x32_bf16(a, b1, acc[rt][1], 0, 0, 0);
+                }
+            }
+#pragma unroll
+            for (int t = 0; t < 2; ++t) {
+                const int n = wid * 2 + t;
+                const float bias = bp2[n * 16 + l16];
+#pragma unroll
+                for (int rt = 0; rt < 4; ++rt)
+#pragma unroll
+                    for (int r = 0; r < 4; ++r)
+                        p_b[(size_t)(brow + rt * 16 + quad * 4 + r) * HD + n * 16 + l16] =
+                            f2bf(acc[rt][t][r] + bias);
+            }
+        }
+    }
+    }
+    if (coop) grid.sync();
+
+    if (phase_lo <= 3 && 3 <= phase_hi) {
+    for (int it = bid; it < FILLB; it += G) {
+        __syncthreads();
+        int* cnt = (int*)smem;
+        const int* Hb = (const int*)(hist16 + it * NG);
+#pragma unroll
+        for (int k2 = 0; k2 < 10; ++k2) {
+            const int idx = k2 * 256 + tid;
+            if (idx < NG / 8) ((int4*)cnt)[idx] = ((const int4*)Hb)[idx];
+        }
+        __syncthreads();
+        const int base = it * EPB;
+#pragma unroll
+        for (int it2 = 0; it2 < 10; ++it2) {
+            const int e0 = base + it2 * 256 + tid;
+            const int s0 = ei[e0];
+            const int d0 = ei[NE + e0];
+            const int o = atomicAdd(&cnt[d0 >> 1], 1 << ((d0 & 1) * 16));
+            const int p = (o >> ((d0 & 1) * 16)) & 0xFFFF;
+            if (p < CAP) pad[d0 * CAP + p] = (unsigned short)s0;
+        }
+    }
+    }
+    if (coop) grid.sync();
+
+    if (phase_lo <= 4 && 4 <= phase_hi) {
+    for (int it = bid; it < AGG_ITEMS; it += G) {
+        const int row = it * 4 + wid;
+        float acc2[8] = {0.f, 0.f, 0.f, 0.f, 0.f, 0.f, 0.f, 0.f};
+        const int cnt2 = min(cursor[row], CAP);
+        const size_t rb = (size_t)row * CAP;
+        for (int i = quad * 4; i < cnt2; i += 16) {
+            const ushort4 q = *(const ushort4*)&pad[rb + i];
+            int r0 = q.x, r1 = q.y, r2 = q.z, r3 = q.w;
+            const bool v1 = (i + 1) < cnt2, v2 = (i + 2) < cnt2, v3 = (i + 3) < cnt2;
+            r1 = v1 ? r1 : r0;  r2 = v2 ? r2 : r0;  r3 = v3 ? r3 : r0;
+            const float s1 = v1 ? 1.f : 0.f, s2 = v2 ? 1.f : 0.f, s3 = v3 ? 1.f : 0.f;
+            const s16x8 g0 = *(const s16x8*)&g[(size_t)r0 * HD + l16 * 8];
+            const s16x8 g1 = *(const s16x8*)&g[(size_t)r1 * HD + l16 * 8];
+            const s16x8 g2 = *(const s16x8*)&g[(size_t)r2 * HD + l16 * 8];
+            const s16x8 g3 = *(const s16x8*)&g[(size_t)r3 * HD + l16 * 8];
+            const unsigned* d0 = (const unsigned*)&g0;
+            const unsigned* d1 = (const unsigned*)&g1;
+            const unsigned* d2 = (const unsigned*)&g2;
+            const unsigned* d3 = (const unsigned*)&g3;
+#pragma unroll
+            for (int k = 0; k < 4; ++k) {
+                acc2[2 * k]     += bfpair_lo(d0[k]);
+                acc2[2 * k + 1] += bfpair_hi(d0[k]);
+                acc2[2 * k]     = fmaf(bfpair_lo(d1[k]), s1, acc2[2 * k]);
+                acc2[2 * k + 1] = fmaf(bfpair_hi(d1[k]), s1, acc2[2 * k + 1]);
+                acc2[2 * k]     = fmaf(bfpair_lo(d2[k]), s2, acc2[2 * k]);
+                acc2[2 * k + 1] = fmaf(bfpair_hi(d2[k]), s2, acc2[2 * k + 1]);
+                acc2[2 * k]     = fmaf(bfpair_lo(d3[k]), s3, acc2[2 * k]);
+                acc2[2 * k + 1] = fmaf(bfpair_hi(d3[k]), s3, acc2[2 * k + 1]);
+            }
+        }
+#pragma unroll
+        for (int k = 0; k < 8; ++k) {
+            acc2[k] += __shfl_xor(acc2[k], 16);
+            acc2[k] += __shfl_xor(acc2[k], 32);
+        }
+        if (lane < 16) {
+            unsigned o[4];
+#pragma unroll
+            for (int k = 0; k < 4; ++k)
+                o[k] = (unsigned)f2bf(acc2[2 * k]) | ((unsigned)f2bf(acc2[2 * k + 1]) << 16);
+            *(int4*)&aggb[(size_t)row * HD + lane * 8] = *(int4*)o;
+        }
+    }
+    }
+    if (coop) grid.sync();
+
+    if (phase_lo <= 5 && 5 <= phase_hi) {
+    for (int it = bid; it < SAGE_ITEMS; it += G) {
+        __syncthreads();
+        const int brow = it * 64;
+        unsigned short* XA = (unsigned short*)smem;
+#pragma unroll
+        for (int s = 0; s < 4; ++s) {
+            const int slot = s * 256 + tid;
+            const int r  = slot >> 4;
+            const int cv = slot & 15;
+            *(s16x8*)&XA[r * 136 + cv * 8] = *(const s16x8*)&p_b[(size_t)(brow + r) * HD + cv * 8];
+        }
+        __syncthreads();
+
+        f32x4 acc[4][2];
+#pragma unroll
+        for (int rt = 0; rt < 4; ++rt) { acc[rt][0] = Z; acc[rt][1] = Z; }
 #pragma unroll
         for (int c = 0; c < 4; ++c) {
-            const s16x8 b = *(const s16x8*)&wfc[(c * 64 + lane) * 8];
-            const s16x8 a = *(const s16x8*)&XA[(wid * 16 + l16) * 136 + c * 32 + quad * 8];
-            co = __builtin_amdgcn_mfma_f32_16x16x32_bf16(a, b, co, 0, 0, 0);
-        }
-        if (l16 < OD) {
-            const float bias = bfc[l16];
-#pragma unroll
-            for (int r = 0; r < 4; ++r) {
-                const int row = brow + wid * 16 + quad * 4 + r;
-                out[(size_t)row * OD + l16] = co[r] + bias;
-            }
-        }
+            const s16x8 br0 = *(const s16x8*)&w1r[(((wid * 2) * 4 + c) * 64 + lane) * 8];
+            const s16x8 br1 = *(const s16x8*)&w1r[(((wid * 2 + 1) * 4 + c) * 64 + lane) * 8];
+            const s16x8 bl0 = *(const s16x8*)&w1l[(((wid * 2) * 4 + c) * 64 + lane) * 8];
+            const s16x8 bl1 = *(const s16x8*)&w1l[(((wid * 2 + 1) * 4 + c) * 64 + lane) * 8];
+#pragma unroll
+            for (int rt = 0; rt < 4; ++rt) {
+                const s16x8 ap = *(const s16x8*)&XA[(rt * 16 + l16) * 136 + c * 32 + quad * 8];
+                const s16x8 ag = *(const s16x8*)&aggb[(size_t)(brow + rt * 16 + l16) * HD + c * 32 + quad * 8];
+                acc[rt][0] = __builtin_amdgcn_mfma_f32_16x16x32_bf16(ap, br0, acc[rt][0], 0, 0, 0);
+                acc[rt][0] = __builtin_amdgcn_mfma_f32_16x16x32_bf16(ag, bl0, acc[rt][0], 0, 0, 0);
+                acc[rt][1] = __builtin_amdgcn_mfma_f32_16x16x32_bf16(ap, br1, acc[rt][1], 0, 0, 0);
+                acc[rt][1] = __builtin_amdgcn_mfma_f32_16x16x32_bf16(ag, bl1, acc[rt][1], 0, 0, 0);
+            }
+        }
+        __syncthreads();
+#pragma unroll
+        for (int t = 0; t < 2; ++t) {
+            const int n = wid * 2 + t;
+            const float bias = b1l[n * 16 + l16];
+#pragma unroll
+            for (int rt = 0; rt < 4; ++rt)
+#pragma unroll
+                for (int r = 0; r < 4; ++r)
+                    XA[(rt * 16 + quad * 4 + r) * 136 + n * 16 + l16] =
+                        f2bf(fmaxf(acc[rt][t][r] + bias, 0.f));
+        }
+        __syncthreads();
+#pragma unroll
+        for (int rt = 0; rt < 4; ++rt) { acc[rt][0] = Z; acc[rt][1] = Z; }
+#pragma unroll
+        for (int c = 0; c < 4; ++c) {
+            const s16x8 br0 = *(const s16x8*)&w2r[(((wid * 2) * 4 + c) * 64 + lane) * 8];
+            const s16x8 br1 = *(const s16x8*)&w2r[(((wid * 2 + 1) * 4 + c) * 64 + lane) * 8];
+            const s16x8 bl0 = *(const s16x8*)&w2l[(((wid * 2) * 4 + c) * 64 + lane) * 8];
+            const s16x8 bl1 = *(const s16x8*)&w2l[(((wid * 2 + 1) * 4 + c) * 64 + lane) * 8];
+#pragma unroll
+            for (int rt = 0; rt < 4; ++rt) {
+                const s16x8 ap = *(const s16x8*)&XA[(rt * 16 + l16) * 136 + c * 32 + quad * 8];
+                const s16x8 ag = *(const s16x8*)&aggb[(size_t)(brow + rt * 16 + l16) * HD + c * 32 + quad * 8];
+                acc[rt][0] = __builtin_amdgcn_mfma_f32_16x16x32_bf16(ap, br0, acc[rt][0], 0, 0, 0);
+                acc[rt][0] = __builtin_amdgcn_mfma_f32_16x16x32_bf16(ag, bl0, acc[rt][0], 0, 0, 0);
+                acc[rt][1] = __builtin_amdgcn_mfma_f32_16x16x32_bf16(ap, br1, acc[rt][1], 0, 0, 0);
+                acc[rt][1] = __builtin_amdgcn_mfma_f32_16x16x32_bf16(ag, bl1, acc[rt][1], 0, 0, 0);
+            }
+        }
+        __syncthreads();
+#pragma unroll
+        for (int t = 0; t < 2; ++t) {
+            const int n = wid * 2 + t;
+            const float bias = b2l[n * 16 + l16];
+#pragma unroll
+            for (int rt = 0; rt < 4; ++rt)
+#pragma unroll
+                for (int r = 0; r < 4; ++r)
+                    XA[(rt * 16 + quad * 4 + r) * 136 + n * 16 + l16] =
+                        f2bf(fmaxf(acc[rt][t][r] + bias, 0.f));
+        }
+        __syncthreads();
+        {
+            f32x4 co = Z;
+#pragma unroll
+            for (int c = 0; c < 4; ++c) {
+                const s16x8 b = *(const s16x8*)&wfc[(c * 64 + lane) * 8];
+                const s16x8 a = *(const s16x8*)&XA[(wid * 16 + l16) * 136 + c * 32 + quad * 8];
+                co = __builtin_amdgcn_mfma_f32_16x16x32_bf16(a, b, co, 0, 0, 0);
+            }
+            if (l16 < OD) {
+                const float bias = bfc[l16];
+#pragma unroll
+                for (int r = 0; r < 4; ++r) {
+                    const int row = brow + wid * 16 + quad * 4 + r;
+                    out[(size_t)row * OD + l16] = co[r] + bias;
+                }
+            }
+        }
+    }
     }
 }
 
@@ -658,22 +627,62 @@
     unsigned short* wswz   = (unsigned short*)(ws + 5120000);
     int*            cursor = (int*)(ws + 5345280);
     unsigned short* hist16 = (unsigned short*)(ws + 5425280);
-    unsigned short* pad    = (unsigned short*)(ws + 10425280);
-    unsigned short* agg_b  = (unsigned short*)(ws + 14265280);
-
-    swz_kernel<<<(TOT_SWZ + AGGPAD * HD) / 256, 256, 0, stream>>>(
-        Wp1, Wp2, W1l, W1r, W2l, W2r, Wfc, Wg1, Wg2, wswz, agg_b);
-
-    genefill_kernel<<<GENE_TILES + FILLB, 256, 0, stream>>>(
-        xg, wswz, bg1, bg2, g_b, ei, hist16);
-
-    scan_kernel<<<(NG + 255) / 256, 256, 0, stream>>>(hist16, cursor);
-
-    placepat_kernel<<<FILLB + PAT2B, 256, 0, stream>>>(
-        ei, hist16, pad, xp, wswz, bp1, bp2, b1l, b2l, bfc, out);
-
-    agg_kernel<<<NG / 4, 256, 0, stream>>>(cursor, pad, g_b, agg_b);
-
-    sage64_kernel<<<SAGE64B, 256, 0, stream>>>(
-        xp, agg_b, wswz, bp1, bp2, b1l, b2l, bfc, out);
+    unsigned short* pad    = (unsigned short*)(ws + 15425280);
+    unsigned short* p_b    = (unsigned short*)(ws + 19265280);
+    unsigned short* agg_b  = (unsigned short*)(ws + 24393472);
+
+    static int s_maxBlocks = -1;
+    if (s_maxBlocks < 0) {
+        int mb = 0;
+        if (hipOccupancyMaxActiveBlocksPerMultiprocessor(
+                &mb, mega_kernel, 256, (size_t)SMEM_BYTES) != hipSuccess)
+            mb = 0;
+        s_maxBlocks = mb;
+    }
+
+    bool done = false;
+    if (s_maxBlocks >= 2) {
+        int plo = 0, phi = 5;
+        const int grid = s_maxBlocks * 256;
+        void* args[] = {
+            (void*)&xp, (void*)&xg, (void*)&ei,
+            (void*)&bp1, (void*)&bp2, (void*)&b1l, (void*)&b2l, (void*)&bfc,
+            (void*)&bg1, (void*)&bg2,
+            (void*)&Wp1, (void*)&Wp2, (void*)&W1l, (void*)&W1r, (void*)&W2l,
+            (void*)&W2r, (void*)&Wfc, (void*)&Wg1, (void*)&Wg2,
+            (void*)&wswz, (void*)&g_b, (void*)&hist16, (void*)&cursor,
+            (void*)&pad, (void*)&p_b, (void*)&agg_b, (void*)&out,
+            (void*)&plo, (void*)&phi
+        };
+        done = (hipLaunchCooperativeKernel((void*)mega_kernel, dim3(grid),
+                                           dim3(256), args, SMEM_BYTES,
+                                           stream) == hipSuccess);
+    }
+
+    if (!done) {
+        mega_kernel<<<456, 256, 0, stream>>>(
+            xp, xg, ei, bp1, bp2, b1l, b2l, bfc, bg1, bg2,
+            Wp1, Wp2, W1l, W1r, W2l, W2r, Wfc, Wg1, Wg2,
+            wswz, g_b, hist16, cursor, pad, p_b, agg_b, out, 0, 0);
+        mega_kernel<<<P1_ITEMS, 256, SMEM_BYTES, stream>>>(
+            xp, xg, ei, bp1, bp2, b1l, b2l, bfc, bg1, bg2,
+            Wp1, Wp2, W1l, W1r, W2l, W2r, Wfc, Wg1, Wg2,
+            wswz, g_b, hist16, cursor, pad, p_b, agg_b, out, 1, 1);
+        mega_kernel<<<P2_ITEMS, 256, SMEM_BYTES, stream>>>(
+            xp, xg, ei, bp1, bp2, b1l, b2l, bfc, bg1, bg2,
+            Wp1, Wp2, W1l, W1r, W2l, W2r, Wfc, Wg1, Wg2,
+            wswz, g_b, hist16, cursor, pad, p_b, agg_b, out, 2, 2);
+        mega_kernel<<<FILLB, 256, SMEM_BYTES, stream>>>(
+            xp, xg, ei, bp1, bp2, b1l, b2l, bfc, bg1, bg2,
+            Wp1, Wp2, W1l, W1r, W2l, W2r, Wfc, Wg1, Wg2,
+            wswz, g_b, hist16, cursor, pad, p_b, agg_b, out, 3, 3);
+        mega_kernel<<<AGG_ITEMS, 256, 0, stream>>>(
+            xp, xg, ei, bp1, bp2, b1l, b2l, bfc, bg1, bg2,
+            Wp1, Wp2, W1l, W1r, W2l, W2r, Wfc, Wg1, Wg2,
+            wswz, g_b, hist16, cursor, pad, p_b, agg_b, out, 4, 4);
+        mega_kernel<<<SAGE_ITEMS, 256, SMEM_BYTES, stream>>>(
+            xp, xg, ei, bp1, bp2, b1l, b2l, bfc, bg1, bg2,
+            Wp1, Wp2, W1l, W1r, W2l, W2r, Wfc, Wg1, Wg2,
+            wswz, g_b, hist16, cursor, pad, p_b, agg_b, out, 5, 5);
+    }
 }
```

After: 555.9 us. +219.5%, slower.
